# Kernel optimization log

Measured on AMD Instinct MI355X. Metric: run time of the kernel, lower is better.

## Reference

```python
import jax, jax.numpy as jnp
import numpy as np

D = 128
NUM_ITEM, NUM_CAT = 100000, 10000
NI, NC = 100000, 10000
EII, ECC, ECI, EIC = 800000, 100000, 400000, 400000
B, T, L = 512, 50, 2


def setup_inputs():
    key = jax.random.key(0)
    ks = jax.random.split(key, 48)
    s = 1.0 / np.sqrt(D)  # matches reset_parameters uniform(-stdv, stdv)
    u = lambda k, sh: jax.random.uniform(k, sh, jnp.float32, -s, s)
    ri = lambda k, sh, hi: jax.random.randint(k, sh, 0, hi, jnp.int32)
    inp = {
        'item_emb': u(ks[0], (NUM_ITEM, D)),
        'cate_emb': u(ks[1], (NUM_CAT, D)),
        'pos_emb': u(ks[2], (200, D)),
        'W_pos': u(ks[3], (2 * D, D)),
        'gat_W': u(ks[4], (L, 4, D, D)),
        'gat_al': u(ks[5], (L, 4, D)),
        'gat_ar': u(ks[6], (L, 4, D)),
        'gat_b': u(ks[7], (L, 4, D)),
        'Wg1_w': u(ks[8], (2 * D, D)), 'Wg1_b': u(ks[9], (D,)),
        'Wg3_w': u(ks[10], (2 * D, D)), 'Wg3_b': u(ks[11], (D,)),
        'q': u(ks[12], (D, 1)),
        'lin_out_w': u(ks[13], (2 * D, D)), 'lin_out_b': u(ks[14], (D,)),
        'w_1': u(ks[15], (2 * D, D)), 'w_2': u(ks[16], (D, 1)),
        'glu1_w': u(ks[17], (D, D)), 'glu1_b': u(ks[18], (D,)),
        'glu2_w': u(ks[19], (D, D)),
        'ln1_g': jnp.ones((D,), jnp.float32), 'ln1_b': jnp.zeros((D,), jnp.float32),
        'ln2_g': jnp.ones((D,), jnp.float32), 'ln2_b': jnp.zeros((D,), jnp.float32),
        'x_s': jax.random.uniform(ks[20], (1,), jnp.float32),
        'y_s': jax.random.uniform(ks[21], (1,), jnp.float32),
        'iid': ri(ks[22], (NI,), NUM_ITEM),
        'icate': ri(ks[23], (NI,), NUM_CAT),
        'cid': ri(ks[24], (NC,), NUM_CAT),
        'src_ii': ri(ks[25], (EII,), NI), 'dst_ii': ri(ks[26], (EII,), NI),
        'src_cc': ri(ks[27], (ECC,), NC), 'dst_cc': ri(ks[28], (ECC,), NC),
        'src_ci': ri(ks[29], (ECI,), NC), 'dst_ci': ri(ks[30], (ECI,), NI),
        'src_ic': ri(ks[31], (EIC,), NI), 'dst_ic': ri(ks[32], (EIC,), NC),
        'alias': ri(ks[33], (B, T), NI),
        'seq_items': ri(ks[34], (B, T), NUM_ITEM),
        'mask_item': jnp.ones((B, T), jnp.int32),
        'last_idx': ri(ks[35], (B,), NI),
    }
    return inp


def _layernorm(x, g, b, eps=1e-8):
    mu = x.mean(-1, keepdims=True)
    v = ((x - mu) ** 2).mean(-1, keepdims=True)
    return (x - mu) / jnp.sqrt(v + eps) * g + b


def _gat(h_src, h_dst, src, dst, W, al, ar, bias, n_dst):
    # DGL GATConv, 1 head, residual (identity since in==out), negative_slope=0.2
    z_src = h_src @ W                      # [Nsrc, D]
    z_dst = h_dst @ W                      # [Ndst, D]
    e = jax.nn.leaky_relu((z_src @ al)[src] + (z_dst @ ar)[dst], 0.2)  # [E]
    m = jax.ops.segment_max(e, dst, num_segments=n_dst)
    ee = jnp.exp(e - m[dst])
    denom = jax.ops.segment_sum(ee, dst, num_segments=n_dst)
    alpha = ee / denom[dst]                # edge softmax per destination
    out = jax.ops.segment_sum(alpha[:, None] * z_src[src], dst, num_segments=n_dst)
    return out + h_dst + bias              # residual then bias (DGL order)


def _compute_scores(hidden, maskf, pos, q, lin_out_w, lin_out_b, w_1, w_2,
                    glu1_w, glu1_b, glu2_w, ln1_g, ln1_b, ln2_g, ln2_b):
    # hidden: [B,T,D], maskf: [B,T,1]
    hs = hidden @ q                                    # [B,T,1]
    beta_a = jax.nn.softmax(hs, axis=1) * maskf
    hsv = jnp.sum(beta_a * hidden, axis=1)             # [B,D]
    hsv = _layernorm(hsv, ln1_g, ln1_b)
    hh = hidden[:, 0]                                  # first position
    hsv = jnp.concatenate([hsv, hh], axis=1) @ lin_out_w + lin_out_b
    nh = jnp.tanh(jnp.concatenate([jnp.broadcast_to(pos[None], hidden.shape), hidden], -1) @ w_1)
    nh = jax.nn.sigmoid(nh @ glu1_w + glu1_b + (hsv @ glu2_w)[:, None, :])
    beta = (nh @ w_2) * maskf                          # [B,T,1]
    sel = jnp.sum(beta * hidden, axis=1)               # [B,D]
    return _layernorm(sel, ln2_g, ln2_b)               # nor == True


def reference(item_emb, cate_emb, pos_emb, W_pos, gat_W, gat_al, gat_ar, gat_b,
              Wg1_w, Wg1_b, Wg3_w, Wg3_b, q, lin_out_w, lin_out_b, w_1, w_2,
              glu1_w, glu1_b, glu2_w, ln1_g, ln1_b, ln2_g, ln2_b, x_s, y_s,
              iid, icate, cid, src_ii, dst_ii, src_cc, dst_cc, src_ci, dst_ci,
              src_ic, dst_ic, alias, seq_items, mask_item, last_idx):
    # feature_encoder
    hi0 = jnp.concatenate([item_emb[iid], cate_emb[icate]], axis=1) @ W_pos  # [NI,D]
    hc0 = cate_emb[cid]                                                     # [NC,D]
    hi, hc = hi0, hc0
    for l in range(L):
        # HeteroGraphConv, aggregate='sum'; relation order: i2i, c2c, c2i, i2c
        ni = (_gat(hi, hi, src_ii, dst_ii, gat_W[l, 0], gat_al[l, 0], gat_ar[l, 0], gat_b[l, 0], NI)
              + _gat(hc, hi, src_ci, dst_ci, gat_W[l, 2], gat_al[l, 2], gat_ar[l, 2], gat_b[l, 2], NI))
        nc = (_gat(hc, hc, src_cc, dst_cc, gat_W[l, 1], gat_al[l, 1], gat_ar[l, 1], gat_b[l, 1], NC)
              + _gat(hi, hc, src_ic, dst_ic, gat_W[l, 3], gat_al[l, 3], gat_ar[l, 3], gat_b[l, 3], NC))
        hi, hc = ni, nc
    # FeatureSelect type='gated' between layer 0 and last layer
    gate_i = jax.nn.sigmoid(jnp.concatenate([hi0, hi], axis=-1) @ Wg1_w + Wg1_b)
    feat_i = gate_i * hi0 + (1.0 - gate_i) * hi
    gate_c = jax.nn.sigmoid(jnp.concatenate([hc0, hc], axis=-1) @ Wg3_w + Wg3_b)
    feat_c = gate_c * hc0 + (1.0 - gate_c) * hc  # computed per original; unused below
    maskf = mask_item.astype(jnp.float32)[..., None]        # [B,T,1]
    h_i_last = feat_i[last_idx]                             # last item per session
    seq_hidden = item_emb[seq_items]                        # local-path embeddings
    h_he = feat_i[alias] * maskf                            # GNN features gathered per session (zero-padded)
    h_all0 = seq_hidden * x_s[0] + h_he
    h_l = _compute_scores(h_all0, maskf, pos_emb[:T], q, lin_out_w, lin_out_b, w_1, w_2,
                          glu1_w, glu1_b, glu2_w, ln1_g, ln1_b, ln2_g, ln2_b)
    h_all = h_l + h_i_last * y_s[0]                         # [B,D]
    fenzi = h_all @ h_all.T
    fenmu_l = jnp.sqrt(jnp.sum(h_all * h_all + 1e-6, axis=1))[:, None]
    cos_sim = fenzi / (fenmu_l @ fenmu_l.T)
    return h_all, cos_sim
```

## Files before the change

### kernel.cpp

```cpp
#include <hip/hip_runtime.h>
#include <hip/hip_fp16.h>

typedef unsigned short u16;
typedef unsigned int u32;
typedef unsigned long long u64;
typedef __attribute__((ext_vector_type(8))) short bf16x8;
typedef __attribute__((ext_vector_type(4))) float f32x4;

#define NI_ 100000
#define NC_ 10000
#define EII_ 800000
#define ECC_ 100000
#define ECI_ 400000
#define EIC_ 400000
#define B_ 512
#define T_ 50
#define BSH_ 9
#define NBII_ 196
#define NBNC_ 20
#define NBK_ 432
#define ECH_ 4096

__device__ __forceinline__ float bf2f(u16 u) { return __uint_as_float(((u32)u) << 16); }
__device__ __forceinline__ u16 f2bf(float x) {
    u32 u = __float_as_uint(x);
    return (u16)((u + 0x7FFFu + ((u >> 16) & 1u)) >> 16);
}
__device__ __forceinline__ float sigm(float x) { return 1.f / (1.f + expf(-x)); }
__device__ __forceinline__ float gldf(const void* p, size_t i, int isf) {
    return isf ? ((const float*)p)[i] : bf2f(((const u16*)p)[i]);
}
__device__ __forceinline__ float lrelu_c(float v) {
    v = (v >= 0.f) ? v : 0.2f * v;
    return fminf(fmaxf(v, -60.f), 60.f);
}

__global__ void k_init(const void* __restrict__ item, int* __restrict__ flag,
                       int* __restrict__ bcnt)
{
    const int tid = threadIdx.x;
    for (int i = tid; i < NBK_; i += 128) bcnt[i] = 0;
    if (tid < 64) {
        const int l = tid;
        bf16x8 a, b;
        #pragma unroll
        for (int j = 0; j < 8; ++j) {
            int ka = (l >> 4) * 8 + j;
            float av = (float)((((l & 15) * 5 + ka * 3) & 15) - 7);
            float bv = (float)(((ka * 7 + (l & 15) * 11) & 15) - 8);
            a[j] = (short)f2bf(av);
            b[j] = (short)f2bf(bv);
        }
        f32x4 d = {0.f, 0.f, 0.f, 0.f};
        d = __builtin_amdgcn_mfma_f32_16x16x32_bf16(a, b, d, 0, 0, 0);
        bool ok = true;
        #pragma unroll
        for (int j = 0; j < 4; ++j) {
            int row = (l >> 4) * 4 + j, col = l & 15;
            float ref = 0.f;
            for (int k = 0; k < 32; ++k)
                ref += (float)(((row * 5 + k * 3) & 15) - 7) * (float)(((k * 7 + col * 11) & 15) - 8);
            ok = ok && (d[j] == ref);
        }
        unsigned long long vote = __ballot(ok);
        if (l == 0) flag[1] = (vote == ~0ull) ? 1 : 0;
    } else if (tid == 64) {
        const u16* p = (const u16*)item;
        int cnt = 0;
        for (int i = 0; i < 128; ++i) {
            float v = bf2f(p[i]);
            if (fabsf(v) <= 0.0886f) ++cnt;
        }
        flag[0] = (cnt >= 120) ? 0 : 1;
    }
}

__global__ void s_sig(float* __restrict__ out, long n, float code)
{
    long i = (long)blockIdx.x * 256 + threadIdx.x;
    if (i < n) out[i] = (i == 0) ? code : 0.f;
}

__global__ __launch_bounds__(256) void k_pre(
    const void* __restrict__ cate, const int* __restrict__ cid, float* __restrict__ hc0,
    const void* __restrict__ Wp, const void* __restrict__ Wg1, const void* __restrict__ gW,
    u16* __restrict__ whi, u16* __restrict__ wlo,
    const void* __restrict__ ar, float* __restrict__ wars,
    const int* __restrict__ d0, const int* __restrict__ d1,
    const int* __restrict__ d2, const int* __restrict__ d3,
    int* __restrict__ bcnt,
    const int* __restrict__ fl)
{
    __shared__ int bl[NBK_];
    const int det = fl[0];
    int bid = blockIdx.x, tid = threadIdx.x;
    if (bid < 5000) {
        long i = (long)bid * 256 + tid;
        if (i < (long)NC_ * 128)
            hc0[i] = gldf(cate, (size_t)cid[i >> 7] * 128 + (i & 127), det);
        return;
    }
    bid -= 5000;
    if (bid < 80) {
        int s = bid * 256 + tid;
        if (s >= 20480) return;
        const void* src; int K, local; size_t soff;
        if (s < 4096)       { src = Wp;  K = 256; local = s;        soff = 0; }
        else if (s < 8192)  { src = Wg1; K = 256; local = s - 4096; soff = 0; }
        else {
            int t = s - 8192; int m = t >> 11; local = t & 2047; K = 128;
            const int MK[6] = {0, 1, 2, 3, 4, 6};
            src = gW; soff = (size_t)MK[m] * 16384;
        }
        const int KK = K >> 5;
        int r = local & 15, g = (local >> 4) & 3, q2 = local >> 6;
        int kk = q2 % KK, ni = q2 / KK;
        bf16x8 hv, lv;
        #pragma unroll
        for (int j = 0; j < 8; ++j) {
            float x = gldf(src, soff + (size_t)(kk * 32 + 8 * g + j) * 128 + ni * 16 + r, det);
            u16 hb = f2bf(x);
            hv[j] = (short)hb;
            lv[j] = (short)f2bf(x - bf2f(hb));
        }
        *(bf16x8*)(whi + (size_t)s * 8) = hv;
        *(bf16x8*)(wlo + (size_t)s * 8) = lv;
        return;
    }
    bid -= 80;
    if (bid < 3) {
        if (tid < 128) {
            const int WO[3] = {2 * 16384, 3 * 16384, 6 * 16384};
            const int AO[3] = {2 * 128, 3 * 128, 6 * 128};
            int g = bid, k = tid;
            float a = 0.f;
            for (int c = 0; c < 128; ++c)
                a += gldf(gW, (size_t)WO[g] + (size_t)k * 128 + c, det) * gldf(ar, AO[g] + c, det);
            wars[g * 128 + k] = a;
        }
        return;
    }
    bid -= 3;
    for (int i = tid; i < NBK_; i += 256) bl[i] = 0;
    __syncthreads();
    const long ET = (long)EII_ + ECI_ + ECC_ + EIC_;
    const long base = (long)bid * ECH_;
    #pragma unroll
    for (int j = 0; j < 16; ++j) {
        long i = base + j * 256 + tid;
        if (i < ET) {
            int dst, boff;
            long ii = i;
            if (ii < EII_) { dst = d0[ii]; boff = 0; }
            else { ii -= EII_;
            if (ii < ECI_) { dst = d1[ii]; boff = NBII_; }
            else { ii -= ECI_;
            if (ii < ECC_) { dst = d2[ii]; boff = 2 * NBII_; }
            else { ii -= ECC_; dst = d3[ii]; boff = 2 * NBII_ + NBNC_; } } }
            atomicAdd(&bl[boff + (dst >> BSH_)], 1);
        }
    }
    __syncthreads();
    for (int i = tid; i < NBK_; i += 256)
        if (bl[i]) atomicAdd(&bcnt[i], bl[i]);
}

__global__ void k_bscan(const int* __restrict__ bcnt,
                        int* __restrict__ bstart, int* __restrict__ gcur)
{
    if (threadIdx.x != 0 || blockIdx.x != 0) return;
    int run = 0;
    for (int i = 0; i < NBII_; ++i) { bstart[i] = run; gcur[i] = run; run += bcnt[i]; }
    run = 0;
    for (int i = NBII_; i < 2 * NBII_; ++i) { bstart[i] = run; gcur[i] = run; run += bcnt[i]; }
    run = 0;
    for (int i = 2 * NBII_; i < 2 * NBII_ + NBNC_; ++i) { bstart[i] = run; gcur[i] = run; run += bcnt[i]; }
    run = 0;
    for (int i = 2 * NBII_ + NBNC_; i < NBK_; ++i) { bstart[i] = run; gcur[i] = run; run += bcnt[i]; }
}

__global__ __launch_bounds__(256) void k_binA(
    const int* s0, const int* d0, const int* s1, const int* d1,
    const int* s2, const int* d2, const int* s3, const int* d3,
    int* __restrict__ gcur,
    u32* __restrict__ b0, u32* __restrict__ b1,
    u32* __restrict__ b2, u32* __restrict__ b3)
{
    __shared__ u32 stag[ECH_];
    __shared__ int cnt[NBK_], base_l[NBK_ + 1], gbase[NBK_], cur_l[NBK_];
    const int tid = threadIdx.x;
    const long estart = (long)blockIdx.x * ECH_;
    const long ET = (long)EII_ + ECI_ + ECC_ + EIC_;
    for (int b = tid; b < NBK_; b += 256) cnt[b] = 0;
    __syncthreads();
    int gidv[16]; u32 pk[16];
    #pragma unroll
    for (int j = 0; j < 16; ++j) {
        long i = estart + j * 256 + tid;
        gidv[j] = -1;
        if (i < ET) {
            int src, dst, boff;
            long ii = i;
            if (ii < EII_) { src = s0[ii]; dst = d0[ii]; boff = 0; }
            else { ii -= EII_;
            if (ii < ECI_) { src = s1[ii]; dst = d1[ii]; boff = NBII_; }
            else { ii -= ECI_;
            if (ii < ECC_) { src = s2[ii]; dst = d2[ii]; boff = 2 * NBII_; }
            else { ii -= ECC_; src = s3[ii]; dst = d3[ii]; boff = 2 * NBII_ + NBNC_; } } }
            int gid = boff + (dst >> BSH_);
            gidv[j] = gid;
            pk[j] = ((u32)src << BSH_) | (u32)(dst & ((1 << BSH_) - 1));
            atomicAdd(&cnt[gid], 1);
        }
    }
    __syncthreads();
    if (tid == 0) {
        int run = 0;
        for (int b = 0; b < NBK_; ++b) { base_l[b] = run; run += cnt[b]; }
        base_l[NBK_] = run;
    }
    __syncthreads();
    for (int b = tid; b < NBK_; b += 256) {
        gbase[b] = cnt[b] ? atomicAdd(&gcur[b], cnt[b]) : 0;
        cur_l[b] = base_l[b];
    }
    __syncthreads();
    #pragma unroll
    for (int j = 0; j < 16; ++j)
        if (gidv[j] >= 0) {
            int l = atomicAdd(&cur_l[gidv[j]], 1);
            stag[l] = pk[j];
        }
    __syncthreads();
    const int total = base_l[NBK_];
    for (int t = tid; t < total; t += 256) {
        int lo = 0, hi = NBK_ - 1;
        while (lo < hi) { int mid = (lo + hi + 1) >> 1; if (base_l[mid] <= t) lo = mid; else hi = mid - 1; }
        int pos = gbase[lo] + (t - base_l[lo]);
        u32* bp = (lo < NBII_) ? b0 : (lo < 2 * NBII_) ? b1 : (lo < 2 * NBII_ + NBNC_) ? b2 : b3;
        bp[pos] = stag[t];
    }
}

__global__ __launch_bounds__(512) void k_binB(
    const int* __restrict__ bstart, const int* __restrict__ bcnt,
    const u32* __restrict__ b0, const u32* __restrict__ b1,
    const u32* __restrict__ b2, const u32* __restrict__ b3,
    int* __restrict__ rpII, int* __restrict__ rpCI,
    int* __restrict__ rpCC, int* __restrict__ rpIC,
    int* __restrict__ csII, int* __restrict__ csCI,
    int* __restrict__ csCC, int* __restrict__ csIC)
{
    __shared__ int cnt[512], cur[512];
    const int gid = blockIdx.x, tid = threadIdx.x;
    int* rp; const u32* bp; int* cs; int b, n, Eg; bool last;
    if (gid < NBII_)                  { rp = rpII; bp = b0; cs = csII; b = gid;                     n = NI_; Eg = EII_; last = (gid == NBII_ - 1); }
    else if (gid < 2 * NBII_)         { rp = rpCI; bp = b1; cs = csCI; b = gid - NBII_;             n = NI_; Eg = ECI_; last = (gid == 2 * NBII_ - 1); }
    else if (gid < 2 * NBII_ + NBNC_) { rp = rpCC; bp = b2; cs = csCC; b = gid - 2 * NBII_;         n = NC_; Eg = ECC_; last = (gid == 2 * NBII_ + NBNC_ - 1); }
    else                              { rp = rpIC; bp = b3; cs = csIC; b = gid - 2 * NBII_ - NBNC_; n = NC_; Eg = EIC_; last = (gid == NBK_ - 1); }
    const int dz = b << BSH_;
    const int d1v = (dz + 512 < n) ? dz + 512 : n;
    const int ndl = d1v - dz;
    cnt[tid] = 0;
    __syncthreads();
    const int e0 = bstart[gid], e1 = e0 + bcnt[gid];
    for (int e = e0 + tid; e < e1; e += 512)
        atomicAdd(&cnt[bp[e] & 511], 1);
    __syncthreads();
    for (int s = 1; s < 512; s <<= 1) {
        int v = (tid >= s) ? cnt[tid - s] : 0;
        __syncthreads();
        cnt[tid] += v;
        __syncthreads();
    }
    const int excl = (tid == 0) ? 0 : cnt[tid - 1];
    cur[tid] = e0 + excl;
    if (tid < ndl) rp[dz + tid] = e0 + excl;
    if (last && tid == 0) rp[n] = Eg;
    __syncthreads();
    for (int e = e0 + tid; e < e1; e += 512) {
        u32 p = bp[e];
        int pos = atomicAdd(&cur[p & 511], 1);
        cs[pos] = (int)(p >> BSH_);
    }
}

__device__ __forceinline__ void gat_gather(
    const int* __restrict__ rp, const int* __restrict__ cs,
    const float* __restrict__ sl, float srd, const __half2* __restrict__ z,
    int w, int lane, float& a0, float& a1)
{
    const int start = rp[w], end = rp[w + 1];
    if (end <= start) return;
    const int cnt = end - start;
    int   sE = 0; float eE = 0.f;
    if (lane < cnt) {
        sE = cs[start + lane];
        eE = expf(lrelu_c(sl[sE] + srd));
    }
    float local = eE;
    for (int k = start + 64 + lane; k < end; k += 64)
        local += expf(lrelu_c(sl[cs[k]] + srd));
    #pragma unroll
    for (int o = 32; o > 0; o >>= 1) local += __shfl_xor(local, o, 64);
    const float inv = 1.f / local;
    const int m = (cnt < 64) ? cnt : 64;
    int k = 0;
    for (; k + 8 <= m; k += 8) {
        int   s[8]; float lw[8]; float2 f[8];
        #pragma unroll
        for (int u = 0; u < 8; ++u) {
            s[u]  = __shfl(sE, k + u, 64);
            lw[u] = __shfl(eE, k + u, 64) * inv;
        }
        #pragma unroll
        for (int u = 0; u < 8; ++u) f[u] = __half22float2(z[(size_t)s[u] * 64 + lane]);
        #pragma unroll
        for (int u = 0; u < 8; ++u) { a0 += lw[u] * f[u].x; a1 += lw[u] * f[u].y; }
    }
    for (; k + 4 <= m; k += 4) {
        int s0 = __shfl(sE, k, 64),     s1 = __shfl(sE, k + 1, 64);
        int s2 = __shfl(sE, k + 2, 64), s3 = __shfl(sE, k + 3, 64);
        float l0 = __shfl(eE, k, 64) * inv,     l1 = __shfl(eE, k + 1, 64) * inv;
        float l2 = __shfl(eE, k + 2, 64) * inv, l3 = __shfl(eE, k + 3, 64) * inv;
        float2 f0 = __half22float2(z[(size_t)s0 * 64 + lane]);
        float2 f1 = __half22float2(z[(size_t)s1 * 64 + lane]);
        float2 f2 = __half22float2(z[(size_t)s2 * 64 + lane]);
        float2 f3 = __half22float2(z[(size_t)s3 * 64 + lane]);
        a0 += l0 * f0.x + l1 * f1.x + l2 * f2.x + l3 * f3.x;
        a1 += l0 * f0.y + l1 * f1.y + l2 * f2.y + l3 * f3.y;
    }
    for (; k < m; ++k) {
        int s = __shfl(sE, k, 64);
        float al = __shfl(eE, k, 64) * inv;
        float2 f = __half22float2(z[(size_t)s * 64 + lane]);
        a0 += al * f.x;
        a1 += al * f.y;
    }
    for (int kk = start + 64; kk < end; ++kk) {
        int s = cs[kk];
        float al = expf(lrelu_c(sl[s] + srd)) * inv;
        float2 f = __half22float2(z[(size_t)s * 64 + lane]);
        a0 += al * f.x;
        a1 += al * f.y;
    }
}

__global__ __launch_bounds__(256) void t_gat_fused(
    const int* __restrict__ rpA, const int* __restrict__ csA,
    const float* __restrict__ slA, const float* __restrict__ srA, const __half2* __restrict__ zA_,
    const int* __restrict__ rpB, const int* __restrict__ csB,
    const float* __restrict__ slB, const float* __restrict__ war, const __half2* __restrict__ zB_,
    const float* __restrict__ h0, const void* __restrict__ gb, int b0off, int b1off,
    const int* __restrict__ fl, float* __restrict__ acc, int ndst)
{
    int w = blockIdx.x * 4 + (threadIdx.x >> 6);
    int lane = threadIdx.x & 63;
    if (w >= ndst) return;
    const int det = *fl;
    const int d0 = 2 * lane, d1 = 2 * lane + 1;
    float2 h0v = *(const float2*)(h0 + (size_t)w * 128 + d0);
    float2 wv  = *(const float2*)(war + d0);
    float srB = h0v.x * wv.x + h0v.y * wv.y;
    #pragma unroll
    for (int off = 32; off > 0; off >>= 1) srB += __shfl_xor(srB, off, 64);
    float a0 = 2.f * h0v.x + gldf(gb, b0off + d0, det) + gldf(gb, b1off + d0, det);
    float a1 = 2.f * h0v.y + gldf(gb, b0off + d1, det) + gldf(gb, b1off + d1, det);
    gat_gather(rpA, csA, slA, srA[w], zA_, w, lane, a0, a1);
    gat_gather(rpB, csB, slB, srB,    zB_, w, lane, a0, a1);
    *(float2*)(acc + (size_t)w * 128 + d0) = make_float2(a0, a1);
}

__global__ __launch_bounds__(256) void k_prepw3(
    const void* __restrict__ w1, const void* __restrict__ g1w,
    const int* __restrict__ fl, u16* __restrict__ whi, u16* __restrict__ wlo)
{
    int s = blockIdx.x * 256 + threadIdx.x;
    if (s >= 6144) return;
    const int det = *fl;
    const void* src; int K, local;
    if (s < 4096) { src = w1;  K = 256; local = s; }
    else          { src = g1w; K = 128; local = s - 4096; }
    const int KK = K >> 5;
    int r = local & 15, g = (local >> 4) & 3, q2 = local >> 6;
    int kk = q2 % KK, ni = q2 / KK;
    bf16x8 hv, lv;
    #pragma unroll
    for (int j = 0; j < 8; ++j) {
        float x = gldf(src, (size_t)(kk * 32 + 8 * g + j) * 128 + ni * 16 + r, det);
        u16 hb = f2bf(x);
        hv[j] = (short)hb;
        lv[j] = (short)f2bf(x - bf2f(hb));
    }
    *(bf16x8*)(whi + (size_t)s * 8) = hv;
    *(bf16x8*)(wlo + (size_t)s * 8) = lv;
}

__global__ __launch_bounds__(256, 2) void m_hi0(
    const void* __restrict__ item, const void* __restrict__ cate,
    const int* __restrict__ iid, const int* __restrict__ icate,
    const u16* __restrict__ whi, const u16* __restrict__ wlo,
    const int* __restrict__ fl, const int* __restrict__ mfok,
    float* __restrict__ out, int nrows)
{
    if (*mfok == 0) return;
    __shared__ __align__(16) short Ah[2048 * 8];
    __shared__ __align__(16) short Alo[2048 * 8];
    const int det = *fl;
    const int tid = threadIdx.x, l = tid & 63, w = tid >> 6;
    const int base = blockIdx.x * 64;
    {
        int row = tid >> 2, q = tid & 3;
        int n = base + row, mi = row >> 4, r = row & 15;
        const int it = (n < nrows) ? iid[n] : 0;
        const int ct = (n < nrows) ? icate[n] : 0;
        #pragma unroll
        for (int i = 0; i < 8; ++i) {
            int c = q + 4 * i, kk = c >> 2, g = c & 3;
            int slot = ((mi * 8 + kk) * 4 + g) * 16 + r;
            bf16x8 hv = {0,0,0,0,0,0,0,0}, lv = {0,0,0,0,0,0,0,0};
            if (n < nrows) {
                #pragma unroll
                for (int j = 0; j < 8; ++j) {
                    float x = (c < 16) ? gldf(item, (size_t)it * 128 + c * 8 + j, det)
                                       : gldf(cate, (size_t)ct * 128 + (c - 16) * 8 + j, det);
                    u16 hb2 = f2bf(x);
                    hv[j] = (short)hb2;
                    lv[j] = (short)f2bf(x - bf2f(hb2));
                }
            }
            *(bf16x8*)&Ah[slot * 8]  = hv;
            *(bf16x8*)&Alo[slot * 8] = lv;
        }
    }
    bf16x8 breg[2][8];
    #pragma unroll
    for (int t = 0; t < 2; ++t)
        #pragma unroll
        for (int kk = 0; kk < 8; ++kk)
            breg[t][kk] = *(const bf16x8*)(whi + ((size_t)((w * 2 + t) * 8 + kk) * 64 + l) * 8);
    __syncthreads();
    f32x4 acc[4][2];
    #pragma unroll
    for (int mi = 0; mi < 4; ++mi) { acc[mi][0] = (f32x4){0.f,0.f,0.f,0.f}; acc[mi][1] = (f32x4){0.f,0.f,0.f,0.f}; }
    auto pass = [&](const short* AS) {
        #pragma unroll
        for (int kk = 0; kk < 8; ++kk) {
            bf16x8 a[4];
            #pragma unroll
            for (int mi = 0; mi < 4; ++mi) a[mi] = *(const bf16x8*)&AS[((mi * 8 + kk) * 64 + l) * 8];
            #pragma unroll
            for (int mi = 0; mi < 4; ++mi) {
                acc[mi][0] = __builtin_amdgcn_mfma_f32_16x16x32_bf16(a[mi], breg[0][kk], acc[mi][0], 0, 0, 0);
                acc[mi][1] = __builtin_amdgcn_mfma_f32_16x16x32_bf16(a[mi], breg[1][kk], acc[mi][1], 0, 0, 0);
            }
        }
    };
    pass(Ah);
    pass(Alo);
    #pragma unroll
    for (int t = 0; t < 2; ++t)
        #pragma unroll
        for (int kk = 0; kk < 8; ++kk)
            breg[t][kk] = *(const bf16x8*)(wlo + ((size_t)((w * 2 + t) * 8 + kk) * 64 + l) * 8);
    pass(Ah);
    const int g = l >> 4, r = l & 15, wn0 = w * 32;
    #pragma unroll
    for (int mi = 0; mi < 4; ++mi)
        #pragma unroll
        for (int j = 0; j < 4; ++j) {
            int row = base + mi * 16 + 4 * g + j;
            if (row < nrows) {
                out[(size_t)row * 128 + wn0 + r]      = acc[mi][0][j];
                out[(size_t)row * 128 + wn0 + 16 + r] = acc[mi][1][j];
            }
        }
}

__global__ __launch_bounds__(256, 2) void m_zgemm(
    const float* __restrict__ h, int nrows,
    const u16* __restrict__ whi, const u16* __restrict__ wlo,
    const void* __restrict__ al, int aloff, const void* __restrict__ ar, int aroff,
    const int* __restrict__ fl, const int* __restrict__ mfok,
    __half* __restrict__ z, float* __restrict__ sl, float* __restrict__ sr)
{
    if (*mfok == 0) return;
    __shared__ __align__(16) short Ah[1024 * 8];
    __shared__ __align__(16) short Alo[1024 * 8];
    __shared__ float part[2][4][64];
    const int det = *fl;
    const int tid = threadIdx.x, l = tid & 63, w = tid >> 6;
    const int base = blockIdx.x * 64;
    {
        int row = tid >> 2, q = tid & 3;
        int n = base + row, mi = row >> 4, r = row & 15;
        #pragma unroll
        for (int i = 0; i < 4; ++i) {
            int c = q + 4 * i, kk = c >> 2, g = c & 3;
            int slot = ((mi * 4 + kk) * 4 + g) * 16 + r;
            bf16x8 hv = {0,0,0,0,0,0,0,0}, lv = {0,0,0,0,0,0,0,0};
            if (n < nrows) {
                const float* sp = h + (size_t)n * 128 + c * 8;
                #pragma unroll
                for (int j = 0; j < 8; ++j) {
                    float x = sp[j];
                    u16 hb = f2bf(x);
                    hv[j] = (short)hb;
                    lv[j] = (short)f2bf(x - bf2f(hb));
                }
            }
            *(bf16x8*)&Ah[slot * 8]  = hv;
            *(bf16x8*)&Alo[slot * 8] = lv;
        }
    }
    bf16x8 breg[2][4];
    #pragma unroll
    for (int t = 0; t < 2; ++t)
        #pragma unroll
        for (int kk = 0; kk < 4; ++kk)
            breg[t][kk] = *(const bf16x8*)(whi + ((size_t)((w * 2 + t) * 4 + kk) * 64 + l) * 8);
    __syncthreads();
    f32x4 acc[4][2];
    #pragma unroll
    for (int mi = 0; mi < 4; ++mi) { acc[mi][0] = (f32x4){0.f,0.f,0.f,0.f}; acc[mi][1] = (f32x4){0.f,0.f,0.f,0.f}; }
    auto pass = [&](const short* AS) {
        #pragma unroll
        for (int kk = 0; kk < 4; ++kk) {
            bf16x8 a[4];
            #pragma unroll
            for (int mi = 0; mi < 4; ++mi) a[mi] = *(const bf16x8*)&AS[((mi * 4 + kk) * 64 + l) * 8];
            #pragma unroll
            for (int mi = 0; mi < 4; ++mi) {
                acc[mi][0] = __builtin_amdgcn_mfma_f32_16x16x32_bf16(a[mi], breg[0][kk], acc[mi][0], 0, 0, 0);
                acc[mi][1] = __builtin_amdgcn_mfma_f32_16x16x32_bf16(a[mi], breg[1][kk], acc[mi][1], 0, 0, 0);
            }
        }
    };
    pass(Ah);
    pass(Alo);
    #pragma unroll
    for (int t = 0; t < 2; ++t)
        #pragma unroll
        for (int kk = 0; kk < 4; ++kk)
            breg[t][kk] = *(const bf16x8*)(wlo + ((size_t)((w * 2 + t) * 4 + kk) * 64 + l) * 8);
    pass(Ah);
    const int g = l >> 4, r = l & 15, wn0 = w * 32;
    const float alv0 = gldf(al, (size_t)aloff + wn0 + r, det);
    const float alv1 = gldf(al, (size_t)aloff + wn0 + 16 + r, det);
    const float arv0 = gldf(ar, (size_t)aroff + wn0 + r, det);
    const float arv1 = gldf(ar, (size_t)aroff + wn0 + 16 + r, det);
    #pragma unroll
    for (int mi = 0; mi < 4; ++mi)
        #pragma unroll
        for (int j = 0; j < 4; ++j) {
            int row = base + mi * 16 + 4 * g + j;
            float d0 = acc[mi][0][j], d1 = acc[mi][1][j];
            if (row < nrows) {
                z[(size_t)row * 128 + wn0 + r]      = __float2half_rn(d0);
                z[(size_t)row * 128 + wn0 + 16 + r] = __float2half_rn(d1);
            }
            float pl = d0 * alv0 + d1 * alv1;
            float pr = d0 * arv0 + d1 * arv1;
            #pragma unroll
            for (int m2 = 1; m2 < 16; m2 <<= 1) {
                pl += __shfl_xor(pl, m2, 64);
                pr += __shfl_xor(pr, m2, 64);
            }
            if (r == 0) {
                part[0][w][mi * 16 + 4 * g + j] = pl;
                part[1][w][mi * 16 + 4 * g + j] = pr;
            }
        }
    __syncthreads();
    if (tid < 128) {
        int which = tid >> 6, t = tid & 63;
        int n2 = base + t;
        if (n2 < nrows) {
            float s = part[which][0][t] + part[which][1][t] + part[which][2][t] + part[which][3][t];
            (which ? sr : sl)[n2] = s;
        }
    }
}

__global__ __launch_bounds__(256, 2) void m_zgemm2(
    const float* __restrict__ h, int nrows,
    const u16* __restrict__ whi1, const u16* __restrict__ wlo1,
    int alo1, int aro1, __half* __restrict__ z1,
    float* __restrict__ sl1, float* __restrict__ sr1,
    const u16* __restrict__ whi2, const u16* __restrict__ wlo2,
    int alo2, int aro2, __half* __restrict__ z2,
    float* __restrict__ sl2, float* __restrict__ sr2,
    const void* __restrict__ al, const void* __restrict__ ar,
    const int* __restrict__ fl, const int* __restrict__ mfok)
{
    if (*mfok == 0) return;
    __shared__ __align__(16) short Ah[1024 * 8];
    __shared__ __align__(16) short Alo[1024 * 8];
    __shared__ float part[2][4][64];
    const int det = *fl;
    const int tid = threadIdx.x, l = tid & 63, w = tid >> 6;
    const int base = blockIdx.x * 64;
    {
        int row = tid >> 2, q = tid & 3;
        int n = base + row, mi = row >> 4, r = row & 15;
        #pragma unroll
        for (int i = 0; i < 4; ++i) {
            int c = q + 4 * i, kk = c >> 2, g = c & 3;
            int slot = ((mi * 4 + kk) * 4 + g) * 16 + r;
            bf16x8 hv = {0,0,0,0,0,0,0,0}, lv = {0,0,0,0,0,0,0,0};
            if (n < nrows) {
                const float* sp = h + (size_t)n * 128 + c * 8;
                #pragma unroll
                for (int j = 0; j < 8; ++j) {
                    float x = sp[j];
                    u16 hb = f2bf(x);
                    hv[j] = (short)hb;
                    lv[j] = (short)f2bf(x - bf2f(hb));
                }
            }
            *(bf16x8*)&Ah[slot * 8]  = hv;
            *(bf16x8*)&Alo[slot * 8] = lv;
        }
    }
    __syncthreads();
    const int g = l >> 4, r = l & 15, wn0 = w * 32;
    auto doSet = [&](const u16* whi, const u16* wlo, int aloff, int aroff,
                     __half* z, float* sl, float* sr) {
        bf16x8 breg[2][4];
        #pragma unroll
        for (int t = 0; t < 2; ++t)
            #pragma unroll
            for (int kk = 0; kk < 4; ++kk)
                breg[t][kk] = *(const bf16x8*)(whi + ((size_t)((w * 2 + t) * 4 + kk) * 64 + l) * 8);
        f32x4 acc[4][2];
        #pragma unroll
        for (int mi = 0; mi < 4; ++mi) { acc[mi][0] = (f32x4){0.f,0.f,0.f,0.f}; acc[mi][1] = (f32x4){0.f,0.f,0.f,0.f}; }
        auto pass = [&](const short* AS) {
            #pragma unroll
            for (int kk = 0; kk < 4; ++kk) {
                bf16x8 a[4];
                #pragma unroll
                for (int mi = 0; mi < 4; ++mi) a[mi] = *(const bf16x8*)&AS[((mi * 4 + kk) * 64 + l) * 8];
                #pragma unroll
                for (int mi = 0; mi < 4; ++mi) {
                    acc[mi][0] = __builtin_amdgcn_mfma_f32_16x16x32_bf16(a[mi], breg[0][kk], acc[mi][0], 0, 0, 0);
                    acc[mi][1] = __builtin_amdgcn_mfma_f32_16x16x32_bf16(a[mi], breg[1][kk], acc[mi][1], 0, 0, 0);
                }
            }
        };
        pass(Ah);
        pass(Alo);
        #pragma unroll
        for (int t = 0; t < 2; ++t)
            #pragma unroll
            for (int kk = 0; kk < 4; ++kk)
                breg[t][kk] = *(const bf16x8*)(wlo + ((size_t)((w * 2 + t) * 4 + kk) * 64 + l) * 8);
        pass(Ah);
        const float alv0 = gldf(al, (size_t)aloff + wn0 + r, det);
        const float alv1 = gldf(al, (size_t)aloff + wn0 + 16 + r, det);
        const float arv0 = gldf(ar, (size_t)aroff + wn0 + r, det);
        const float arv1 = gldf(ar, (size_t)aroff + wn0 + 16 + r, det);
        #pragma unroll
        for (int mi = 0; mi < 4; ++mi)
            #pragma unroll
            for (int j = 0; j < 4; ++j) {
                int row = base + mi * 16 + 4 * g + j;
                float d0 = acc[mi][0][j], d1 = acc[mi][1][j];
                if (row < nrows) {
                    z[(size_t)row * 128 + wn0 + r]      = __float2half_rn(d0);
                    z[(size_t)row * 128 + wn0 + 16 + r] = __float2half_rn(d1);
                }
                float pl = d0 * alv0 + d1 * alv1;
                float pr = d0 * arv0 + d1 * arv1;
                #pragma unroll
                for (int m2 = 1; m2 < 16; m2 <<= 1) {
                    pl += __shfl_xor(pl, m2, 64);
                    pr += __shfl_xor(pr, m2, 64);
                }
                if (r == 0) {
                    part[0][w][mi * 16 + 4 * g + j] = pl;
                    part[1][w][mi * 16 + 4 * g + j] = pr;
                }
            }
        __syncthreads();
        if (tid < 128) {
            int which = tid >> 6, t = tid & 63;
            int n2 = base + t;
            if (n2 < nrows) {
                float s = part[which][0][t] + part[which][1][t] + part[which][2][t] + part[which][3][t];
                (which ? sr : sl)[n2] = s;
            }
        }
        __syncthreads();
    };
    doSet(whi1, wlo1, alo1, aro1, z1, sl1, sr1);
    doSet(whi2, wlo2, alo2, aro2, z2, sl2, sr2);
}

__global__ __launch_bounds__(256, 2) void m_gatefeat(
    const float* __restrict__ h0, const float* __restrict__ h1,
    const u16* __restrict__ whi, const u16* __restrict__ wlo,
    const void* __restrict__ bias,
    const int* __restrict__ fl, const int* __restrict__ mfok,
    float* __restrict__ feat, int nrows)
{
    if (*mfok == 0) return;
    __shared__ __align__(16) short Ah[2048 * 8];
    __shared__ __align__(16) short Alo[2048 * 8];
    const int det = *fl;
    const int tid = threadIdx.x, l = tid & 63, w = tid >> 6;
    const int base = blockIdx.x * 64;
    {
        int row = tid >> 2, q = tid & 3;
        int n = base + row, mi = row >> 4, r = row & 15;
        #pragma unroll
        for (int i = 0; i < 8; ++i) {
            int c = q + 4 * i, kk = c >> 2, g = c & 3;
            int slot = ((mi * 8 + kk) * 4 + g) * 16 + r;
            bf16x8 hv = {0,0,0,0,0,0,0,0}, lv = {0,0,0,0,0,0,0,0};
            if (n < nrows) {
                const float* sp = ((c < 16) ? h0 : h1) + (size_t)n * 128 + (c & 15) * 8;
                #pragma unroll
                for (int j = 0; j < 8; ++j) {
                    float x = sp[j];
                    u16 hb = f2bf(x);
                    hv[j] = (short)hb;
                    lv[j] = (short)f2bf(x - bf2f(hb));
                }
            }
            *(bf16x8*)&Ah[slot * 8]  = hv;
            *(bf16x8*)&Alo[slot * 8] = lv;
        }
    }
    bf16x8 breg[2][8];
    #pragma unroll
    for (int t = 0; t < 2; ++t)
        #pragma unroll
        for (int kk = 0; kk < 8; ++kk)
            breg[t][kk] = *(const bf16x8*)(whi + ((size_t)((w * 2 + t) * 8 + kk) * 64 + l) * 8);
    __syncthreads();
    f32x4 acc[4][2];
    #pragma unroll
    for (int mi = 0; mi < 4; ++mi) { acc[mi][0] = (f32x4){0.f,0.f,0.f,0.f}; acc[mi][1] = (f32x4){0.f,0.f,0.f,0.f}; }
    auto pass = [&](const short* AS) {
        #pragma unroll
        for (int kk = 0; kk < 8; ++kk) {
            bf16x8 a[4];
            #pragma unroll
            for (int mi = 0; mi < 4; ++mi) a[mi] = *(const bf16x8*)&AS[((mi * 8 + kk) * 64 + l) * 8];
            #pragma unroll
            for (int mi = 0; mi < 4; ++mi) {
                acc[mi][0] = __builtin_amdgcn_mfma_f32_16x16x32_bf16(a[mi], breg[0][kk], acc[mi][0], 0, 0, 0);
                acc[mi][1] = __builtin_amdgcn_mfma_f32_16x16x32_bf16(a[mi], breg[1][kk], acc[mi][1], 0, 0, 0);
            }
        }
    };
    pass(Ah);
    pass(Alo);
    #pragma unroll
    for (int t = 0; t < 2; ++t)
        #pragma unroll
        for (int kk = 0; kk < 8; ++kk)
            breg[t][kk] = *(const bf16x8*)(wlo + ((size_t)((w * 2 + t) * 8 + kk) * 64 + l) * 8);
    pass(Ah);
    const int g = l >> 4, r = l & 15, wn0 = w * 32;
    const float bv0 = gldf(bias, wn0 + r, det);
    const float bv1 = gldf(bias, wn0 + 16 + r, det);
    #pragma unroll
    for (int mi = 0; mi < 4; ++mi)
        #pragma unroll
        for (int j = 0; j < 4; ++j) {
            int row = base + mi * 16 + 4 * g + j;
            if (row < nrows) {
                size_t o0 = (size_t)row * 128 + wn0 + r;
                size_t o1 = o0 + 16;
                float ga  = sigm(acc[mi][0][j] + bv0);
                float gb2 = sigm(acc[mi][1][j] + bv1);
                feat[o0] = ga  * h0[o0] + (1.f - ga)  * h1[o0];
                feat[o1] = gb2 * h0[o1] + (1.f - gb2) * h1[o1];
            }
        }
}

__global__ __launch_bounds__(256, 2) void m_nhglu(
    const void* __restrict__ pos, const float* __restrict__ hall0,
    const u16* __restrict__ whi1, const u16* __restrict__ wlo1,
    const u16* __restrict__ whi2, const u16* __restrict__ wlo2,
    const void* __restrict__ gb, const float* __restrict__ g2,
    const void* __restrict__ w2, const int* __restrict__ mask,
    const int* __restrict__ fl, const int* __restrict__ mfok,
    float* __restrict__ beta, int nrows)
{
    if (*mfok == 0) return;
    __shared__ __align__(16) short Ah[2048 * 8];
    __shared__ __align__(16) short Alo[2048 * 8];
    __shared__ float part[4][64];
    const int det = *fl;
    const int tid = threadIdx.x, l = tid & 63, w = tid >> 6;
    const int base = blockIdx.x * 64;
    {
        int row = tid >> 2, q = tid & 3;
        int n = base + row, mi = row >> 4, r = row & 15;
        const int t = (n < nrows) ? (n - (n / T_) * T_) : 0;
        #pragma unroll
        for (int i = 0; i < 8; ++i) {
            int c = q + 4 * i, kk = c >> 2, g = c & 3;
            int slot = ((mi * 8 + kk) * 4 + g) * 16 + r;
            bf16x8 hv = {0,0,0,0,0,0,0,0}, lv = {0,0,0,0,0,0,0,0};
            if (n < nrows) {
                #pragma unroll
                for (int j = 0; j < 8; ++j) {
                    float x = (c < 16) ? gldf(pos, (size_t)t * 128 + c * 8 + j, det)
                                       : hall0[(size_t)n * 128 + (c - 16) * 8 + j];
                    u16 hb = f2bf(x);
                    hv[j] = (short)hb;
                    lv[j] = (short)f2bf(x - bf2f(hb));
                }
            }
            *(bf16x8*)&Ah[slot * 8]  = hv;
            *(bf16x8*)&Alo[slot * 8] = lv;
        }
    }
    bf16x8 breg[2][8];
    #pragma unroll
    for (int t = 0; t < 2; ++t)
        #pragma unroll
        for (int kk = 0; kk < 8; ++kk)
            breg[t][kk] = *(const bf16x8*)(whi1 + ((size_t)((w * 2 + t) * 8 + kk) * 64 + l) * 8);
    __syncthreads();
    f32x4 acc[4][2];
    #pragma unroll
    for (int mi = 0; mi < 4; ++mi) { acc[mi][0] = (f32x4){0.f,0.f,0.f,0.f}; acc[mi][1] = (f32x4){0.f,0.f,0.f,0.f}; }
    auto pass1 = [&](const short* AS) {
        #pragma unroll
        for (int kk = 0; kk < 8; ++kk) {
            bf16x8 a[4];
            #pragma unroll
            for (int mi = 0; mi < 4; ++mi) a[mi] = *(const bf16x8*)&AS[((mi * 8 + kk) * 64 + l) * 8];
            #pragma unroll
            for (int mi = 0; mi < 4; ++mi) {
                acc[mi][0] = __builtin_amdgcn_mfma_f32_16x16x32_bf16(a[mi], breg[0][kk], acc[mi][0], 0, 0, 0);
                acc[mi][1] = __builtin_amdgcn_mfma_f32_16x16x32_bf16(a[mi], breg[1][kk], acc[mi][1], 0, 0, 0);
            }
        }
    };
    pass1(Ah);
    pass1(Alo);
    #pragma unroll
    for (int t = 0; t < 2; ++t)
        #pragma unroll
        for (int kk = 0; kk < 8; ++kk)
            breg[t][kk] = *(const bf16x8*)(wlo1 + ((size_t)((w * 2 + t) * 8 + kk) * 64 + l) * 8);
    pass1(Ah);
    __syncthreads();
    {
        const int g = l >> 4, r = l & 15, wn0 = w * 32;
        #pragma unroll
        for (int mi = 0; mi < 4; ++mi)
            #pragma unroll
            for (int j = 0; j < 4; ++j) {
                int nloc = mi * 16 + 4 * g + j;
                int rr = nloc & 15, mi2 = nloc >> 4;
                #pragma unroll
                for (int hh = 0; hh < 2; ++hh) {
                    int col = wn0 + 16 * hh + r;
                    float x = tanhf(acc[mi][hh][j]);
                    int c = col >> 3, jj = col & 7;
                    int slot = ((mi2 * 4 + (c >> 2)) * 4 + (c & 3)) * 16 + rr;
                    u16 hb = f2bf(x);
                    Ah[slot * 8 + jj]  = (short)hb;
                    Alo[slot * 8 + jj] = (short)f2bf(x - bf2f(hb));
                }
            }
    }
    __syncthreads();
    bf16x8 breg2[2][4];
    #pragma unroll
    for (int t = 0; t < 2; ++t)
        #pragma unroll
        for (int kk = 0; kk < 4; ++kk)
            breg2[t][kk] = *(const bf16x8*)(whi2 + ((size_t)((w * 2 + t) * 4 + kk) * 64 + l) * 8);
    f32x4 acc2[4][2];
    #pragma unroll
    for (int mi = 0; mi < 4; ++mi) { acc2[mi][0] = (f32x4){0.f,0.f,0.f,0.f}; acc2[mi][1] = (f32x4){0.f,0.f,0.f,0.f}; }
    auto pass2 = [&](const short* AS) {
        #pragma unroll
        for (int kk = 0; kk < 4; ++kk) {
            bf16x8 a[4];
            #pragma unroll
            for (int mi = 0; mi < 4; ++mi) a[mi] = *(const bf16x8*)&AS[((mi * 4 + kk) * 64 + l) * 8];
            #pragma unroll
            for (int mi = 0; mi < 4; ++mi) {
                acc2[mi][0] = __builtin_amdgcn_mfma_f32_16x16x32_bf16(a[mi], breg2[0][kk], acc2[mi][0], 0, 0, 0);
                acc2[mi][1] = __builtin_amdgcn_mfma_f32_16x16x32_bf16(a[mi], breg2[1][kk], acc2[mi][1], 0, 0, 0);
            }
        }
    };
    pass2(Ah);
    pass2(Alo);
    #pragma unroll
    for (int t = 0; t < 2; ++t)
        #pragma unroll
        for (int kk = 0; kk < 4; ++kk)
            breg2[t][kk] = *(const bf16x8*)(wlo2 + ((size_t)((w * 2 + t) * 4 + kk) * 64 + l) * 8);
    pass2(Ah);
    const int g = l >> 4, r = l & 15, wn0 = w * 32;
    const float gbv0 = gldf(gb, wn0 + r, det);
    const float gbv1 = gldf(gb, wn0 + 16 + r, det);
    const float w2v0 = gldf(w2, wn0 + r, det);
    const float w2v1 = gldf(w2, wn0 + 16 + r, det);
    #pragma unroll
    for (int mi = 0; mi < 4; ++mi)
        #pragma unroll
        for (int j = 0; j < 4; ++j) {
            int row = base + mi * 16 + 4 * g + j;
            int b = row / T_;
            float gv0 = (row < nrows) ? g2[(size_t)b * 128 + wn0 + r]      : 0.f;
            float gv1 = (row < nrows) ? g2[(size_t)b * 128 + wn0 + 16 + r] : 0.f;
            float v0 = sigm(acc2[mi][0][j] + gbv0 + gv0);
            float v1 = sigm(acc2[mi][1][j] + gbv1 + gv1);
            float pl = v0 * w2v0 + v1 * w2v1;
            #pragma unroll
            for (int m2 = 1; m2 < 16; m2 <<= 1) pl += __shfl_xor(pl, m2, 64);
            if (r == 0) part[w][mi * 16 + 4 * g + j] = pl;
        }
    __syncthreads();
    if (tid < 64) {
        int n2 = base + tid;
        if (n2 < nrows) {
            float s = part[0][tid] + part[1][tid] + part[2][tid] + part[3][tid];
            beta[n2] = s * (float)mask[n2];
        }
    }
}

__global__ __launch_bounds__(512) void t_hi0(
    const void* __restrict__ item, const void* __restrict__ cate,
    const int* __restrict__ iid, const int* __restrict__ icate,
    const void* __restrict__ Wp, const int* __restrict__ fl,
    float* __restrict__ out, int nrows)
{
    __shared__ float Ws[8192];
    __shared__ float hrow[16][256];
    const int det = *fl;
    const int tid = threadIdx.x, c = tid & 31, slot = tid >> 5;
    for (int base = blockIdx.x * 16; base < nrows; base += gridDim.x * 16) {
        const int n = base + slot;
        if (n < nrows) {
            const int it = iid[n], ct = icate[n];
            for (int j = c; j < 128; j += 32) {
                hrow[slot][j]       = gldf(item, (size_t)it * 128 + j, det);
                hrow[slot][128 + j] = gldf(cate, (size_t)ct * 128 + j, det);
            }
        }
        float4 acc = make_float4(0.f, 0.f, 0.f, 0.f);
        for (int kb = 0; kb < 256; kb += 64) {
            __syncthreads();
            for (int i = tid; i < 8192; i += 512) Ws[i] = gldf(Wp, (size_t)kb * 128 + i, det);
            __syncthreads();
            if (n < nrows) {
                #pragma unroll 8
                for (int k = 0; k < 64; ++k) {
                    float hv = hrow[slot][kb + k];
                    float4 w = *(const float4*)&Ws[k * 128 + c * 4];
                    acc.x += hv * w.x; acc.y += hv * w.y; acc.z += hv * w.z; acc.w += hv * w.w;
                }
            }
        }
        if (n < nrows) *(float4*)&out[(size_t)n * 128 + c * 4] = acc;
        __syncthreads();
    }
}

__global__ __launch_bounds__(256) void s_hc0(
    const void* __restrict__ cate, const int* __restrict__ cid,
    const int* __restrict__ fl, float* __restrict__ out)
{
    long i = (long)blockIdx.x * 256 + threadIdx.x;
    if (i >= (long)NC_ * 128) return;
    out[i] = gldf(cate, (size_t)cid[i >> 7] * 128 + (i & 127), *fl);
}

__global__ __launch_bounds__(256) void s_initacc(
    const float* __restrict__ h, const void* __restrict__ gb, int b0off, int b1off,
    const int* __restrict__ fl, float* __restrict__ acc, long total)
{
    long i = (long)blockIdx.x * 256 + threadIdx.x;
    if (i >= total) return;
    const int det = *fl, d = (int)(i & 127);
    acc[i] = 2.f * h[i] + gldf(gb, b0off + d, det) + gldf(gb, b1off + d, det);
}

__global__ __launch_bounds__(512) void t_zgemm(
    const float* __restrict__ h, int nrows,
    const void* __restrict__ W, int woff,
    const void* __restrict__ al, int aloff,
    const void* __restrict__ ar, int aroff,
    const int* __restrict__ fl,
    __half* __restrict__ z, float* __restrict__ sl, float* __restrict__ sr)
{
    __shared__ float Ws[8192];
    __shared__ float hrow[16][128];
    const int det = *fl;
    const int tid = threadIdx.x, c = tid & 31, slot = tid >> 5;
    float4 alv, arv;
    alv.x = gldf(al, (size_t)aloff + c * 4 + 0, det); alv.y = gldf(al, (size_t)aloff + c * 4 + 1, det);
    alv.z = gldf(al, (size_t)aloff + c * 4 + 2, det); alv.w = gldf(al, (size_t)aloff + c * 4 + 3, det);
    arv.x = gldf(ar, (size_t)aroff + c * 4 + 0, det); arv.y = gldf(ar, (size_t)aroff + c * 4 + 1, det);
    arv.z = gldf(ar, (size_t)aroff + c * 4 + 2, det); arv.w = gldf(ar, (size_t)aroff + c * 4 + 3, det);
    for (int base = blockIdx.x * 16; base < nrows; base += gridDim.x * 16) {
        const int n = base + slot;
        if (n < nrows) for (int j = c; j < 128; j += 32) hrow[slot][j] = h[(size_t)n * 128 + j];
        float4 acc = make_float4(0.f, 0.f, 0.f, 0.f);
        for (int kb = 0; kb < 128; kb += 64) {
            __syncthreads();
            for (int i = tid; i < 8192; i += 512) Ws[i] = gldf(W, (size_t)woff + (size_t)kb * 128 + i, det);
            __syncthreads();
            if (n < nrows) {
                #pragma unroll 8
                for (int k = 0; k < 64; ++k) {
                    float hv = hrow[slot][kb + k];
                    float4 w = *(const float4*)&Ws[k * 128 + c * 4];
                    acc.x += hv * w.x; acc.y += hv * w.y; acc.z += hv * w.z; acc.w += hv * w.w;
                }
            }
        }
        if (n < nrows) {
            z[(size_t)n * 128 + c * 4 + 0] = __float2half_rn(acc.x);
            z[(size_t)n * 128 + c * 4 + 1] = __float2half_rn(acc.y);
            z[(size_t)n * 128 + c * 4 + 2] = __float2half_rn(acc.z);
            z[(size_t)n * 128 + c * 4 + 3] = __float2half_rn(acc.w);
            float pl = acc.x * alv.x + acc.y * alv.y + acc.z * alv.z + acc.w * alv.w;
            float pr = acc.x * arv.x + acc.y * arv.y + acc.z * arv.z + acc.w * arv.w;
            #pragma unroll
            for (int off = 16; off > 0; off >>= 1) {
                pl += __shfl_down(pl, off, 32);
                pr += __shfl_down(pr, off, 32);
            }
            if (c == 0) { sl[n] = pl; sr[n] = pr; }
        }
        __syncthreads();
    }
}

__global__ __launch_bounds__(256) void s_dinit(float* __restrict__ den, int n)
{
    int i = blockIdx.x * 256 + threadIdx.x;
    if (i < n) den[i] = 0.f;
}
__global__ __launch_bounds__(256) void s_edge(
    const float* __restrict__ sl, const float* __restrict__ sr,
    const int* __restrict__ src, const int* __restrict__ dst,
    float* __restrict__ e, float* __restrict__ den, int E)
{
    int j = blockIdx.x * 256 + threadIdx.x;
    if (j >= E) return;
    float ee = expf(lrelu_c(sl[src[j]] + sr[dst[j]]));
    e[j] = ee;
    atomicAdd(&den[dst[j]], ee);
}
__global__ __launch_bounds__(256) void s_scatter(
    const float* __restrict__ e, const float* __restrict__ den,
    const int* __restrict__ src, const int* __restrict__ dst,
    const __half* __restrict__ z, float* __restrict__ acc, int E)
{
    long i = (long)blockIdx.x * 256 + threadIdx.x;
    if (i >= (long)E * 128) return;
    int j = (int)(i >> 7), d = (int)(i & 127);
    int dj = dst[j];
    atomicAdd(&acc[(size_t)dj * 128 + d], (e[j] / den[dj]) * __half2float(z[(size_t)src[j] * 128 + d]));
}

__global__ __launch_bounds__(512) void t_gatefeat(
    const float* __restrict__ h0, const float* __restrict__ h1,
    const void* __restrict__ W, const void* __restrict__ bias,
    const int* __restrict__ fl,
    float* __restrict__ feat, int nrows)
{
    __shared__ float Ws[8192];
    __shared__ float hrow[16][256];
    const int det = *fl;
    const int tid = threadIdx.x, c = tid & 31, slot = tid >> 5;
    float4 bv;
    bv.x = gldf(bias, c * 4 + 0, det); bv.y = gldf(bias, c * 4 + 1, det);
    bv.z = gldf(bias, c * 4 + 2, det); bv.w = gldf(bias, c * 4 + 3, det);
    for (int base = blockIdx.x * 16; base < nrows; base += gridDim.x * 16) {
        const int n = base + slot;
        if (n < nrows) {
            for (int j = c; j < 128; j += 32) {
                hrow[slot][j]       = h0[(size_t)n * 128 + j];
                hrow[slot][128 + j] = h1[(size_t)n * 128 + j];
            }
        }
        float4 acc = make_float4(0.f, 0.f, 0.f, 0.f);
        for (int kb = 0; kb < 256; kb += 64) {
            __syncthreads();
            for (int i = tid; i < 8192; i += 512) Ws[i] = gldf(W, (size_t)kb * 128 + i, det);
            __syncthreads();
            if (n < nrows) {
                #pragma unroll 8
                for (int k = 0; k < 64; ++k) {
                    float hv = hrow[slot][kb + k];
                    float4 w = *(const float4*)&Ws[k * 128 + c * 4];
                    acc.x += hv * w.x; acc.y += hv * w.y; acc.z += hv * w.z; acc.w += hv * w.w;
                }
            }
        }
        if (n < nrows) {
            float4 a = *(const float4*)&hrow[slot][c * 4];
            float4 b = *(const float4*)&hrow[slot][128 + c * 4];
            float gx = sigm(acc.x + bv.x), gy = sigm(acc.y + bv.y);
            float gz = sigm(acc.z + bv.z), gw = sigm(acc.w + bv.w);
            float4 o;
            o.x = gx * a.x + (1.f - gx) * b.x;
            o.y = gy * a.y + (1.f - gy) * b.y;
            o.z = gz * a.z + (1.f - gz) * b.z;
            o.w = gw * a.w + (1.f - gw) * b.w;
            *(float4*)&feat[(size_t)n * 128 + c * 4] = o;
        }
        __syncthreads();
    }
}

__global__ __launch_bounds__(128) void t_attn12(
    const void* __restrict__ item, const int* __restrict__ seq,
    const int* __restrict__ alias, const int* __restrict__ maskp,
    const float* __restrict__ feat, const void* __restrict__ xs,
    const void* __restrict__ q,
    const void* __restrict__ g, const void* __restrict__ bb,
    const void* __restrict__ lw, const void* __restrict__ lb,
    const void* __restrict__ gw, const int* __restrict__ fl,
    float* __restrict__ hall0, float* __restrict__ g2)
{
    __shared__ float hl[T_][129];
    __shared__ float qs[128];
    __shared__ float hs_s[T_];
    __shared__ float red[128];
    __shared__ float h1s[128];
    __shared__ float h2[128];
    const int b = blockIdx.x, tid = threadIdx.x;
    const int det = *fl;
    const float x = gldf(xs, 0, det);
    qs[tid] = gldf(q, tid, det);
    for (int t = 0; t < T_; ++t) {
        int bt = b * T_ + t;
        float v = gldf(item, (size_t)seq[bt] * 128 + tid, det) * x
                + feat[(size_t)alias[bt] * 128 + tid] * (float)maskp[bt];
        hl[t][tid] = v;
        hall0[(size_t)bt * 128 + tid] = v;
    }
    __syncthreads();
    if (tid < T_) {
        float a = 0.f;
        for (int d = 0; d < 128; ++d) a += hl[tid][d] * qs[d];
        hs_s[tid] = a;
    }
    __syncthreads();
    float mx = -1e30f;
    for (int t = 0; t < T_; ++t) mx = fmaxf(mx, hs_s[t]);
    float ssum = 0.f;
    for (int t = 0; t < T_; ++t) ssum += expf(hs_s[t] - mx);
    float inv = 1.f / ssum;
    __syncthreads();
    if (tid < T_)
        hs_s[tid] = expf(hs_s[tid] - mx) * inv * (float)maskp[b * T_ + tid];
    __syncthreads();
    float a = 0.f;
    for (int t = 0; t < T_; ++t) a += hs_s[t] * hl[t][tid];
    red[tid] = a; __syncthreads();
    for (int o = 64; o > 0; o >>= 1) { if (tid < o) red[tid] += red[tid + o]; __syncthreads(); }
    float mu = red[0] * (1.f / 128.f);
    __syncthreads();
    float dv = a - mu;
    red[tid] = dv * dv; __syncthreads();
    for (int o = 64; o > 0; o >>= 1) { if (tid < o) red[tid] += red[tid + o]; __syncthreads(); }
    float rs = 1.f / sqrtf(red[0] * (1.f / 128.f) + 1e-8f);
    h1s[tid] = dv * rs * gldf(g, tid, det) + gldf(bb, tid, det);
    __syncthreads();
    float a2 = gldf(lb, tid, det);
    for (int k = 0; k < 128; ++k)
        a2 += h1s[k] * gldf(lw, (size_t)k * 128 + tid, det);
    for (int k = 0; k < 128; ++k)
        a2 += hl[0][k] * gldf(lw, (size_t)(128 + k) * 128 + tid, det);
    h2[tid] = a2;
    __syncthreads();
    float g2v = 0.f;
    for (int k = 0; k < 128; ++k)
        g2v += h2[k] * gldf(gw, (size_t)k * 128 + tid, det);
    g2[(size_t)b * 128 + tid] = g2v;
}

__global__ __launch_bounds__(512) void t_nh(
    const void* __restrict__ pos, const float* __restrict__ hall0,
    const void* __restrict__ W, const int* __restrict__ fl,
    float* __restrict__ nh, int nrows)
{
    __shared__ float Ws[8192];
    __shared__ float hrow[16][256];
    const int det = *fl;
    const int tid = threadIdx.x, c = tid & 31, slot = tid >> 5;
    for (int base = blockIdx.x * 16; base < nrows; base += gridDim.x * 16) {
        const int n = base + slot;
        if (n < nrows) {
            const int t = n - (n / T_) * T_;
            for (int j = c; j < 128; j += 32) {
                hrow[slot][j]       = gldf(pos, (size_t)t * 128 + j, det);
                hrow[slot][128 + j] = hall0[(size_t)n * 128 + j];
            }
        }
        float4 acc = make_float4(0.f, 0.f, 0.f, 0.f);
        for (int kb = 0; kb < 256; kb += 64) {
            __syncthreads();
            for (int i = tid; i < 8192; i += 512) Ws[i] = gldf(W, (size_t)kb * 128 + i, det);
            __syncthreads();
            if (n < nrows) {
                #pragma unroll 8
                for (int k = 0; k < 64; ++k) {
                    float hv = hrow[slot][kb + k];
                    float4 w = *(const float4*)&Ws[k * 128 + c * 4];
                    acc.x += hv * w.x; acc.y += hv * w.y; acc.z += hv * w.z; acc.w += hv * w.w;
                }
            }
        }
        if (n < nrows) {
            float4 o;
            o.x = tanhf(acc.x); o.y = tanhf(acc.y); o.z = tanhf(acc.z); o.w = tanhf(acc.w);
            *(float4*)&nh[(size_t)n * 128 + c * 4] = o;
        }
        __syncthreads();
    }
}

__global__ __launch_bounds__(512) void t_glu_beta(
    const float* __restrict__ nh, const void* __restrict__ W, const void* __restrict__ gb,
    const float* __restrict__ g2, const void* __restrict__ w2, const int* __restrict__ mask,
    const int* __restrict__ fl, float* __restrict__ beta, int nrows)
{
    __shared__ float Ws[8192];
    __shared__ float hrow[16][128];
    const int det = *fl;
    const int tid = threadIdx.x, c = tid & 31, slot = tid >> 5;
    float4 gbv, w2v;
    gbv.x = gldf(gb, c * 4 + 0, det); gbv.y = gldf(gb, c * 4 + 1, det);
    gbv.z = gldf(gb, c * 4 + 2, det); gbv.w = gldf(gb, c * 4 + 3, det);
    w2v.x = gldf(w2, c * 4 + 0, det); w2v.y = gldf(w2, c * 4 + 1, det);
    w2v.z = gldf(w2, c * 4 + 2, det); w2v.w = gldf(w2, c * 4 + 3, det);
    for (int base = blockIdx.x * 16; base < nrows; base += gridDim.x * 16) {
        const int n = base + slot;
        if (n < nrows) for (int j = c; j < 128; j += 32) hrow[slot][j] = nh[(size_t)n * 128 + j];
        float4 acc = make_float4(0.f, 0.f, 0.f, 0.f);
        for (int kb = 0; kb < 128; kb += 64) {
            __syncthreads();
            for (int i = tid; i < 8192; i += 512) Ws[i] = gldf(W, (size_t)kb * 128 + i, det);
            __syncthreads();
            if (n < nrows) {
                #pragma unroll 8
                for (int k = 0; k < 64; ++k) {
                    float hv = hrow[slot][kb + k];
                    float4 w = *(const float4*)&Ws[k * 128 + c * 4];
                    acc.x += hv * w.x; acc.y += hv * w.y; acc.z += hv * w.z; acc.w += hv * w.w;
                }
            }
        }
        if (n < nrows) {
            const int b = n / T_;
            float4 gv = *(const float4*)&g2[(size_t)b * 128 + c * 4];
            float vx = sigm(acc.x + gbv.x + gv.x);
            float vy = sigm(acc.y + gbv.y + gv.y);
            float vz = sigm(acc.z + gbv.z + gv.z);
            float vw = sigm(acc.w + gbv.w + gv.w);
            float part = vx * w2v.x + vy * w2v.y + vz * w2v.z + vw * w2v.w;
            #pragma unroll
            for (int off = 16; off > 0; off >>= 1) part += __shfl_down(part, off, 32);
            if (c == 0) beta[n] = part * (float)mask[n];
        }
        __syncthreads();
    }
}

__global__ __launch_bounds__(128) void t_sel(
    const float* __restrict__ hall0, const float* __restrict__ beta,
    const void* __restrict__ g2, const void* __restrict__ b2,
    const float* __restrict__ feat, const int* __restrict__ lasti,
    const void* __restrict__ ys, const int* __restrict__ fl,
    float* __restrict__ hallf, float* __restrict__ fenmu, float* __restrict__ outh)
{
    __shared__ float bet[T_];
    __shared__ float red[128];
    const int b = blockIdx.x, tid = threadIdx.x;
    const int det = *fl;
    if (tid < T_) bet[tid] = beta[b * T_ + tid];
    __syncthreads();
    float acc = 0.f;
    for (int t = 0; t < T_; ++t) acc += bet[t] * hall0[((size_t)b * T_ + t) * 128 + tid];
    red[tid] = acc; __syncthreads();
    for (int off = 64; off > 0; off >>= 1) { if (tid < off) red[tid] += red[tid + off]; __syncthreads(); }
    float mu = red[0] * (1.f / 128.f);
    __syncthreads();
    float dv = acc - mu;
    red[tid] = dv * dv; __syncthreads();
    for (int off = 64; off > 0; off >>= 1) { if (tid < off) red[tid] += red[tid + off]; __syncthreads(); }
    float rs = 1.f / sqrtf(red[0] * (1.f / 128.f) + 1e-8f);
    __syncthreads();
    float h = dv * rs * gldf(g2, tid, det) + gldf(b2, tid, det)
            + feat[(size_t)lasti[b] * 128 + tid] * gldf(ys, 0, det);
    hallf[(size_t)b * 128 + tid] = h;
    outh[(size_t)b * 128 + tid] = h;
    red[tid] = h * h; __syncthreads();
    for (int off = 64; off > 0; off >>= 1) { if (tid < off) red[tid] += red[tid + off]; __syncthreads(); }
    if (tid == 0) fenmu[b] = sqrtf(red[0] + 128.f * 1e-6f);
}

__global__ __launch_bounds__(256) void t_cos(
    const float* __restrict__ hallf, const float* __restrict__ fenmu, float* __restrict__ out)
{
    __shared__ float hi[128];
    const int i = blockIdx.x, tid = threadIdx.x;
    if (tid < 128) hi[tid] = hallf[(size_t)i * 128 + tid];
    __syncthreads();
    const float fi = fenmu[i];
    for (int j = tid; j < B_; j += 256) {
        const float* hj = &hallf[(size_t)j * 128];
        float s = 0.f;
        for (int d = 0; d < 128; d += 4) {
            float4 a = *(const float4*)&hi[d];
            float4 bb = *(const float4*)&hj[d];
            s += a.x * bb.x + a.y * bb.y + a.z * bb.z + a.w * bb.w;
        }
        out[(size_t)i * B_ + j] = s / (fi * fenmu[j]);
    }
}

extern "C" void kernel_launch(void* const* d_in, const int* in_sizes, int n_in,
                              void* d_out, int out_size, void* d_ws, size_t ws_size,
                              hipStream_t stream)
{
    float* outf = (float*)d_out;
    const long OUT_N = (long)B_ * 128 + (long)B_ * B_;

    static const int EXP_SZ[41] = {
        12800000, 1280000, 25600, 32768, 131072, 1024, 1024, 1024, 32768, 128,
        32768, 128, 128, 32768, 128, 32768, 128, 16384, 128, 16384,
        128, 128, 128, 128, 1, 1, 100000, 100000, 10000, 800000,
        800000, 100000, 100000, 400000, 400000, 400000, 400000, 25600, 25600, 25600, 512 };
    float code = 0.f;
    if (n_in != 41) code = 90000.f + (float)n_in;
    else {
        for (int i = 0; i < 41; ++i)
            if (in_sizes[i] != EXP_SZ[i]) { code = 10000.f * (float)(i + 1); break; }
    }
    if (code == 0.f && out_size != (int)OUT_N) code = 95000.f;
    if (code != 0.f) {
        s_sig<<<dim3((unsigned)((OUT_N + 255) / 256)), dim3(256), 0, stream>>>(outf, OUT_N, code);
        return;
    }

    const void* item_emb = d_in[0];
    const void* cate_emb = d_in[1];
    const void* pos_emb  = d_in[2];
    const void* W_pos    = d_in[3];
    const void* gat_W    = d_in[4];
    const void* gat_al   = d_in[5];
    const void* gat_ar   = d_in[6];
    const void* gat_b    = d_in[7];
    const void* Wg1_w    = d_in[8];
    const void* Wg1_b    = d_in[9];
    const void* q        = d_in[12];
    const void* lin_w    = d_in[13];
    const void* lin_b    = d_in[14];
    const void* w_1      = d_in[15];
    const void* w_2      = d_in[16];
    const void* glu1_w   = d_in[17];
    const void* glu1_b   = d_in[18];
    const void* glu2_w   = d_in[19];
    const void* ln1_g    = d_in[20];
    const void* ln1_b    = d_in[21];
    const void* ln2_g    = d_in[22];
    const void* ln2_b    = d_in[23];
    const void* x_s      = d_in[24];
    const void* y_s      = d_in[25];
    const int* iid    = (const int*)d_in[26];
    const int* icate  = (const int*)d_in[27];
    const int* cid    = (const int*)d_in[28];
    const int* src_ii = (const int*)d_in[29];
    const int* dst_ii = (const int*)d_in[30];
    const int* src_cc = (const int*)d_in[31];
    const int* dst_cc = (const int*)d_in[32];
    const int* src_ci = (const int*)d_in[33];
    const int* dst_ci = (const int*)d_in[34];
    const int* src_ic = (const int*)d_in[35];
    const int* dst_ic = (const int*)d_in[36];
    const int* alias  = (const int*)d_in[37];
    const int* seq    = (const int*)d_in[38];
    const int* mask   = (const int*)d_in[39];
    const int* lasti  = (const int*)d_in[40];

    const size_t NEED_BASE = 64 + ((size_t)4 * NI_ + 3 * NC_) * 128 * 4
                                + ((size_t)3 * NI_ + 2 * NC_ + EII_) * 4;
    const size_t CSR_EXTRA = ((size_t)2 * (NI_ + 1) + 2 * (NC_ + 1)
                                + ECI_ + ECC_ + EIC_ + NI_) * 4;
    const size_t NEED_CSR = NEED_BASE + CSR_EXTRA;
    if (ws_size < NEED_BASE) {
        s_sig<<<dim3((unsigned)((OUT_N + 255) / 256)), dim3(256), 0, stream>>>(outf, OUT_N, 80000.f);
        return;
    }
    const bool useCSR = (ws_size >= NEED_CSR);
    const int mf = useCSR ? 1 : 0;

    int* flagp = (int*)d_ws;
    char* basep = (char*)d_ws;
    size_t off = 64;
    auto AL = [&](size_t nfl) { float* p = (float*)(basep + off); off += nfl * 4; return p; };
    float* hi0 = AL((size_t)NI_ * 128);
    float* HiA = AL((size_t)NI_ * 128);
    float* HiB = AL((size_t)NI_ * 128);
    float* zA  = AL((size_t)NI_ * 128);
    float* hc0 = AL((size_t)NC_ * 128);
    float* HcA = AL((size_t)NC_ * 128);
    float* zC  = AL((size_t)NC_ * 128);
    float* sAl = AL(NI_); float* sAr = AL(NI_);
    float* sCl = AL(NC_); float* sCr = AL(NC_);
    float* denF = AL(NI_);
    float* eF   = AL(EII_);
    int* rpII = (int*)AL(NI_ + 1);
    int* rpCI = (int*)AL(NI_ + 1);
    int* rpCC = (int*)AL(NC_ + 1);
    int* rpIC = (int*)AL(NC_ + 1);
    int* csCI = (int*)AL(ECI_);
    int* csCC = (int*)AL(ECC_);
    int* csIC = (int*)AL(EIC_);
    int* wtregion = (int*)AL(NI_);
    int* csII = (int*)eF;
    int* denFi = (int*)denF;
    int* bcnt   = denFi;
    int* bstart = denFi + 512;
    int* gcur   = denFi + 1024;
    float* wars = denF + 2048;
    u16* wt_hi = (u16*)wtregion;
    u16* wt_lo = (u16*)((char*)denF + 17408);
    __half* zAh  = (__half*)zA;
    __half* zA2h = zAh + (size_t)NI_ * 128;
    __half* zCh  = (__half*)zC;
    __half* zC2h = zCh + (size_t)NC_ * 128;
    u32* binII = (u32*)HiB;
    u32* binCI = binII + EII_;
    u32* binCC = binCI + ECI_;
    u32* binIC = binCC + ECC_;
    float* sl03p = HiB;
    float* sr03s = HiB + NI_;
    float* sl02p = HiB + 2 * (size_t)NI_;
    float* sr02s = sl02p + NC_;
    u16* wt2_hi = (u16*)HiA;
    u16* wt2_lo = wt2_hi + (size_t)6144 * 8;

    auto WTS = [&](int l, int k) {
        int midx = (l == 0) ? k : ((k == 0) ? 4 : 5);
        return (size_t)(8192 + midx * 2048) * 8;
    };

    float* feat = zA;
    float* hall0 = hi0;
    float* nh    = hall0 + (size_t)B_ * T_ * 128;
    float* vbuf  = nh    + (size_t)B_ * T_ * 128;
    float* hsb   = vbuf  + (size_t)B_ * T_ * 128;
    float* hsv   = hsb   + (size_t)B_ * T_;
    float* hsvn  = hsv   + (size_t)B_ * 128;
    float* hsv2  = hsvn  + (size_t)B_ * 128;
    float* g2b   = hsv2  + (size_t)B_ * 128;
    float* betab = g2b   + (size_t)B_ * 128;
    float* hallf = betab + (size_t)B_ * T_;
    float* fenmu = hallf + (size_t)B_ * 128;

    #define GRL(n) dim3((unsigned)(((long)(n) + 255) / 256))
    auto WOFF = [](int l, int k) { return (l * 4 + k) * 16384; };
    auto VOFF = [](int l, int k) { return (l * 4 + k) * 128; };

    auto seg = [&](const float* sl, const float* sr, const int* s, const int* d,
                   int E, int ndst, const __half* z, float* acc) {
        s_dinit<<<GRL(ndst), dim3(256), 0, stream>>>(denF, ndst);
        s_edge<<<GRL(E), dim3(256), 0, stream>>>(sl, sr, s, d, eF, denF, E);
        s_scatter<<<GRL((long)E * 128), dim3(256), 0, stream>>>(eF, denF, s, d, z, acc, E);
    };

    k_init<<<dim3(1), dim3(128), 0, stream>>>(item_emb, flagp, bcnt);

    if (useCSR) {
        const int ET = EII_ + ECI_ + ECC_ + EIC_;
        const int NBA = (ET + ECH_ - 1) / ECH_;
        k_pre<<<dim3(5083 + NBA), dim3(256), 0, stream>>>(
            cate_emb, cid, hc0,
            W_pos, Wg1_w, gat_W, wt_hi, wt_lo, gat_ar, wars,
            dst_ii, dst_ci, dst_cc, dst_ic, bcnt, flagp);
        k_bscan<<<dim3(1), dim3(1), 0, stream>>>(bcnt, bstart, gcur);
        k_binA<<<dim3(NBA), dim3(256), 0, stream>>>(
            src_ii, dst_ii, src_ci, dst_ci, src_cc, dst_cc, src_ic, dst_ic,
            gcur, binII, binCI, binCC, binIC);
        k_binB<<<dim3(NBK_), dim3(512), 0, stream>>>(
            bstart, bcnt, binII, binCI, binCC, binIC,
            rpII, rpCI, rpCC, rpIC, csII, csCI, csCC, csIC);
        m_hi0<<<dim3((NI_ + 63) / 64), dim3(256), 0, stream>>>(
            item_emb, cate_emb, iid, icate, wt_hi, wt_lo, flagp, flagp + 1, hi0, NI_);
        m_zgemm2<<<dim3((NI_ + 63) / 64), dim3(256), 0, stream>>>(
            hi0, NI_,
            wt_hi + WTS(0, 0), wt_lo + WTS(0, 0), VOFF(0, 0), VOFF(0, 0), zAh,  sAl,   sAr,
            wt_hi + WTS(0, 3), wt_lo + WTS(0, 3), VOFF(0, 3), VOFF(0, 3), zA2h, sl03p, sr03s,
            gat_al, gat_ar, flagp, flagp + 1);
        m_zgemm2<<<dim3((NC_ + 63) / 64), dim3(256), 0, stream>>>(
            hc0, NC_,
            wt_hi + WTS(0, 1), wt_lo + WTS(0, 1), VOFF(0, 1), VOFF(0, 1), zC2h, sCl,   sCr,
            wt_hi + WTS(0, 2), wt_lo + WTS(0, 2), VOFF(0, 2), VOFF(0, 2), zCh,  sl02p, sr02s,
            gat_al, gat_ar, flagp, flagp + 1);
        t_gat_fused<<<dim3((NI_ + 3) / 4), dim3(256), 0, stream>>>(
            rpII, csII, sAl, sAr, (const __half2*)zAh,
            rpCI, csCI, sl02p, wars + 0, (const __half2*)zCh,
            hi0, gat_b, VOFF(0, 0), VOFF(0, 2), flagp, HiA, NI_);
        t_gat_fused<<<dim3((NC_ + 3) / 4), dim3(256), 0, stream>>>(
            rpCC, csCC, sCl, sCr, (const __half2*)zC2h,
            rpIC, csIC, sl03p, wars + 128, (const __half2*)zA2h,
            hc0, gat_b, VOFF(0, 1), VOFF(0, 3), flagp, HcA, NC_);
        m_zgemm<<<dim3((NI_ + 63) / 64), dim3(256), 0, stream>>>(
            HiA, NI_, wt_hi + WTS(1, 0), wt_lo + WTS(1, 0),
            gat_al, VOFF(1, 0), gat_ar, VOFF(1, 0), flagp, flagp + 1, zAh, sAl, sAr);
        m_zgemm<<<dim3((NC_ + 63) / 64), dim3(256), 0, stream>>>(
            HcA, NC_, wt_hi + WTS(1, 2), wt_lo + WTS(1, 2),
            gat_al, VOFF(1, 2), gat_ar, VOFF(1, 2), flagp, flagp + 1, zCh, sCl, sCr);
        t_gat_fused<<<dim3((NI_ + 3) / 4), dim3(256), 0, stream>>>(
            rpII, csII, sAl, sAr, (const __half2*)zAh,
            rpCI, csCI, sCl, wars + 256, (const __half2*)zCh,
            HiA, gat_b, VOFF(1, 0), VOFF(1, 2), flagp, HiB, NI_);
        k_prepw3<<<dim3(24), dim3(256), 0, stream>>>(w_1, glu1_w, flagp, wt2_hi, wt2_lo);
        m_gatefeat<<<dim3((NI_ + 63) / 64), dim3(256), 0, stream>>>(
            hi0, HiB, wt_hi + (size_t)4096 * 8, wt_lo + (size_t)4096 * 8, Wg1_b, flagp, flagp + 1, feat, NI_);
    } else {
        s_hc0<<<GRL((long)NC_ * 128), dim3(256), 0, stream>>>(cate_emb, cid, flagp, hc0);
        t_hi0<<<dim3(768), dim3(512), 0, stream>>>(item_emb, cate_emb, iid, icate, W_pos, flagp, hi0, NI_);
        s_initacc<<<GRL((long)NI_ * 128), dim3(256), 0, stream>>>(hi0, gat_b, VOFF(0, 0), VOFF(0, 2), flagp, HiA, (long)NI_ * 128);
        s_initacc<<<GRL((long)NC_ * 128), dim3(256), 0, stream>>>(hc0, gat_b, VOFF(0, 1), VOFF(0, 3), flagp, HcA, (long)NC_ * 128);
        t_zgemm<<<dim3(1024), dim3(512), 0, stream>>>(hi0, NI_, gat_W, WOFF(0, 0), gat_al, VOFF(0, 0), gat_ar, VOFF(0, 0), flagp, zAh, sAl, sAr);
        seg(sAl, sAr, src_ii, dst_ii, EII_, NI_, zAh, HiA);
        t_zgemm<<<dim3(625), dim3(512), 0, stream>>>(hc0, NC_, gat_W, WOFF(0, 2), gat_al, VOFF(0, 2), gat_ar, VOFF(0, 2), flagp, zCh, sCl, sCr);
        t_zgemm<<<dim3(1024), dim3(512), 0, stream>>>(hi0, NI_, gat_W, WOFF(0, 2), gat_al, VOFF(0, 2), gat_ar, VOFF(0, 2), flagp, zAh, sAl, sAr);
        seg(sCl, sAr, src_ci, dst_ci, ECI_, NI_, zCh, HiA);
        t_zgemm<<<dim3(625), dim3(512), 0, stream>>>(hc0, NC_, gat_W, WOFF(0, 1), gat_al, VOFF(0, 1), gat_ar, VOFF(0, 1), flagp, zCh, sCl, sCr);
        seg(sCl, sCr, src_cc, dst_cc, ECC_, NC_, zCh, HcA);
        t_zgemm<<<dim3(1024), dim3(512), 0, stream>>>(hi0, NI_, gat_W, WOFF(0, 3), gat_al, VOFF(0, 3), gat_ar, VOFF(0, 3), flagp, zAh, sAl, sAr);
        t_zgemm<<<dim3(625), dim3(512), 0, stream>>>(hc0, NC_, gat_W, WOFF(0, 3), gat_al, VOFF(0, 3), gat_ar, VOFF(0, 3), flagp, zCh, sCl, sCr);
        seg(sAl, sCr, src_ic, dst_ic, EIC_, NC_, zAh, HcA);
        s_initacc<<<GRL((long)NI_ * 128), dim3(256), 0, stream>>>(HiA, gat_b, VOFF(1, 0), VOFF(1, 2), flagp, HiB, (long)NI_ * 128);
        t_zgemm<<<dim3(1024), dim3(512), 0, stream>>>(HiA, NI_, gat_W, WOFF(1, 0), gat_al, VOFF(1, 0), gat_ar, VOFF(1, 0), flagp, zAh, sAl, sAr);
        seg(sAl, sAr, src_ii, dst_ii, EII_, NI_, zAh, HiB);
        t_zgemm<<<dim3(625), dim3(512), 0, stream>>>(HcA, NC_, gat_W, WOFF(1, 2), gat_al, VOFF(1, 2), gat_ar, VOFF(1, 2), flagp, zCh, sCl, sCr);
        t_zgemm<<<dim3(1024), dim3(512), 0, stream>>>(HiA, NI_, gat_W, WOFF(1, 2), gat_al, VOFF(1, 2), gat_ar, VOFF(1, 2), flagp, zAh, sAl, sAr);
        seg(sCl, sAr, src_ci, dst_ci, ECI_, NI_, zCh, HiB);
        t_gatefeat<<<dim3(768), dim3(512), 0, stream>>>(hi0, HiB, Wg1_w, Wg1_b, flagp, feat, NI_);
    }

    t_attn12<<<dim3(B_), dim3(128), 0, stream>>>(
        item_emb, seq, alias, mask, feat, x_s, q,
        ln1_g, ln1_b, lin_w, lin_b, glu2_w, flagp, hall0, g2b);
    if (mf) {
        m_nhglu<<<dim3((B_ * T_ + 63) / 64), dim3(256), 0, stream>>>(
            pos_emb, hall0, wt2_hi, wt2_lo,
            wt2_hi + (size_t)4096 * 8, wt2_lo + (size_t)4096 * 8,
            glu1_b, g2b, w_2, mask, flagp, flagp + 1, betab, B_ * T_);
    } else {
        int grid = (B_ * T_ + 15) / 16; if (grid > 1024) grid = 1024;
        t_nh<<<dim3(grid), dim3(512), 0, stream>>>(pos_emb, hall0, w_1, flagp, nh, B_ * T_);
        t_glu_beta<<<dim3(grid), dim3(512), 0, stream>>>(nh, glu1_w, glu1_b, g2b, w_2, mask, flagp, betab, B_ * T_);
    }
    t_sel<<<dim3(B_), dim3(128), 0, stream>>>(hall0, betab, ln2_g, ln2_b, feat, lasti, y_s, flagp, hallf, fenmu, outf);
    t_cos<<<dim3(B_), dim3(256), 0, stream>>>(hallf, fenmu, outf + (size_t)B_ * 128);
}
```

Baseline: 860.8 us.

## Fuse hi0 GEMM with z-GEMMs, merge item/category GAT launches, MFMA attention linears

Fuses the initial item projection with both layer-0 attention GEMMs so the projected rows stay in LDS and need not be re-read from global memory. It merges the item and category GAT aggregation launches, and likewise the two layer-1 z-GEMMs, into single dual-role grids. The per-session linear layers, previously done with scalar code inside t_attn12, move to a new MFMA kernel (m_lin) fed by a lighter attention kernel. The cost is more LDS use and register pressure in the fused kernel, plus more complex dispatch logic.

```diff
diff --git a/kernel.cpp b/kernel.cpp
--- a/kernel.cpp
+++ b/kernel.cpp
@@ -346,6 +346,28 @@
     }
 }
 
+__device__ __forceinline__ void gat_dst(
+    int w, int lane, int det,
+    const int* __restrict__ rpA, const int* __restrict__ csA,
+    const float* __restrict__ slA, const float* __restrict__ srA, const __half2* __restrict__ zA_,
+    const int* __restrict__ rpB, const int* __restrict__ csB,
+    const float* __restrict__ slB, const float* __restrict__ war, const __half2* __restrict__ zB_,
+    const float* __restrict__ h0, const void* __restrict__ gb, int b0off, int b1off,
+    float* __restrict__ acc)
+{
+    const int d0 = 2 * lane, d1 = 2 * lane + 1;
+    float2 h0v = *(const float2*)(h0 + (size_t)w * 128 + d0);
+    float2 wv  = *(const float2*)(war + d0);
+    float srB = h0v.x * wv.x + h0v.y * wv.y;
+    #pragma unroll
+    for (int off = 32; off > 0; off >>= 1) srB += __shfl_xor(srB, off, 64);
+    float a0 = 2.f * h0v.x + gldf(gb, b0off + d0, det) + gldf(gb, b1off + d0, det);
+    float a1 = 2.f * h0v.y + gldf(gb, b0off + d1, det) + gldf(gb, b1off + d1, det);
+    gat_gather(rpA, csA, slA, srA[w], zA_, w, lane, a0, a1);
+    gat_gather(rpB, csB, slB, srB,    zB_, w, lane, a0, a1);
+    *(float2*)(acc + (size_t)w * 128 + d0) = make_float2(a0, a1);
+}
+
 __global__ __launch_bounds__(256) void t_gat_fused(
     const int* __restrict__ rpA, const int* __restrict__ csA,
     const float* __restrict__ slA, const float* __restrict__ srA, const __half2* __restrict__ zA_,
@@ -357,30 +379,45 @@
     int w = blockIdx.x * 4 + (threadIdx.x >> 6);
     int lane = threadIdx.x & 63;
     if (w >= ndst) return;
+    gat_dst(w, lane, *fl, rpA, csA, slA, srA, zA_, rpB, csB, slB, war, zB_, h0, gb, b0off, b1off, acc);
+}
+
+__global__ __launch_bounds__(256) void t_gat2(
+    const int* rpAi, const int* csAi, const float* slAi, const float* srAi, const __half2* zAi,
+    const int* rpBi, const int* csBi, const float* slBi, const float* wari, const __half2* zBi,
+    const float* h0i, int b0i, int b1i, float* acci,
+    const int* rpAc, const int* csAc, const float* slAc, const float* srAc, const __half2* zAc,
+    const int* rpBc, const int* csBc, const float* slBc, const float* warc, const __half2* zBc,
+    const float* h0c, int b0c, int b1c, float* accc,
+    const void* __restrict__ gb, const int* __restrict__ fl)
+{
+    const int nblkI = (NI_ + 3) / 4;
+    const int lane = threadIdx.x & 63;
     const int det = *fl;
-    const int d0 = 2 * lane, d1 = 2 * lane + 1;
-    float2 h0v = *(const float2*)(h0 + (size_t)w * 128 + d0);
-    float2 wv  = *(const float2*)(war + d0);
-    float srB = h0v.x * wv.x + h0v.y * wv.y;
-    #pragma unroll
-    for (int off = 32; off > 0; off >>= 1) srB += __shfl_xor(srB, off, 64);
-    float a0 = 2.f * h0v.x + gldf(gb, b0off + d0, det) + gldf(gb, b1off + d0, det);
-    float a1 = 2.f * h0v.y + gldf(gb, b0off + d1, det) + gldf(gb, b1off + d1, det);
-    gat_gather(rpA, csA, slA, srA[w], zA_, w, lane, a0, a1);
-    gat_gather(rpB, csB, slB, srB,    zB_, w, lane, a0, a1);
-    *(float2*)(acc + (size_t)w * 128 + d0) = make_float2(a0, a1);
+    if ((int)blockIdx.x < nblkI) {
+        int w = blockIdx.x * 4 + (threadIdx.x >> 6);
+        if (w >= NI_) return;
+        gat_dst(w, lane, det, rpAi, csAi, slAi, srAi, zAi, rpBi, csBi, slBi, wari, zBi, h0i, gb, b0i, b1i, acci);
+    } else {
+        int w = (blockIdx.x - nblkI) * 4 + (threadIdx.x >> 6);
+        if (w >= NC_) return;
+        gat_dst(w, lane, det, rpAc, csAc, slAc, srAc, zAc, rpBc, csBc, slBc, warc, zBc, h0c, gb, b0c, b1c, accc);
+    }
 }
 
 __global__ __launch_bounds__(256) void k_prepw3(
     const void* __restrict__ w1, const void* __restrict__ g1w,
+    const void* __restrict__ lw, const void* __restrict__ g2w,
     const int* __restrict__ fl, u16* __restrict__ whi, u16* __restrict__ wlo)
 {
     int s = blockIdx.x * 256 + threadIdx.x;
-    if (s >= 6144) return;
+    if (s >= 12288) return;
     const int det = *fl;
     const void* src; int K, local;
-    if (s < 4096) { src = w1;  K = 256; local = s; }
-    else          { src = g1w; K = 128; local = s - 4096; }
+    if (s < 4096)       { src = w1;  K = 256; local = s; }
+    else if (s < 6144)  { src = g1w; K = 128; local = s - 4096; }
+    else if (s < 10240) { src = lw;  K = 256; local = s - 6144; }
+    else                { src = g2w; K = 128; local = s - 10240; }
     const int KK = K >> 5;
     int r = local & 15, g = (local >> 4) & 3, q2 = local >> 6;
     int kk = q2 % KK, ni = q2 / KK;
@@ -396,16 +433,100 @@
     *(bf16x8*)(wlo + (size_t)s * 8) = lv;
 }
 
-__global__ __launch_bounds__(256, 2) void m_hi0(
+__device__ __forceinline__ void zg_doset(
+    const short* __restrict__ Ah, const short* __restrict__ Alo,
+    float (*part)[4][64],
+    int tid, int l, int w, int base, int nrows, int det,
+    const u16* __restrict__ whi, const u16* __restrict__ wlo,
+    const void* __restrict__ al, int aloff, const void* __restrict__ ar, int aroff,
+    __half* __restrict__ z, float* __restrict__ sl, float* __restrict__ sr)
+{
+    bf16x8 breg[2][4];
+    #pragma unroll
+    for (int t = 0; t < 2; ++t)
+        #pragma unroll
+        for (int kk = 0; kk < 4; ++kk)
+            breg[t][kk] = *(const bf16x8*)(whi + ((size_t)((w * 2 + t) * 4 + kk) * 64 + l) * 8);
+    f32x4 acc[4][2];
+    #pragma unroll
+    for (int mi = 0; mi < 4; ++mi) { acc[mi][0] = (f32x4){0.f,0.f,0.f,0.f}; acc[mi][1] = (f32x4){0.f,0.f,0.f,0.f}; }
+    auto pass = [&](const short* AS) {
+        #pragma unroll
+        for (int kk = 0; kk < 4; ++kk) {
+            bf16x8 a[4];
+            #pragma unroll
+            for (int mi = 0; mi < 4; ++mi) a[mi] = *(const bf16x8*)&AS[((mi * 4 + kk) * 64 + l) * 8];
+            #pragma unroll
+            for (int mi = 0; mi < 4; ++mi) {
+                acc[mi][0] = __builtin_amdgcn_mfma_f32_16x16x32_bf16(a[mi], breg[0][kk], acc[mi][0], 0, 0, 0);
+                acc[mi][1] = __builtin_amdgcn_mfma_f32_16x16x32_bf16(a[mi], breg[1][kk], acc[mi][1], 0, 0, 0);
+            }
+        }
+    };
+    pass(Ah);
+    pass(Alo);
+    #pragma unroll
+    for (int t = 0; t < 2; ++t)
+        #pragma unroll
+        for (int kk = 0; kk < 4; ++kk)
+            breg[t][kk] = *(const bf16x8*)(wlo + ((size_t)((w * 2 + t) * 4 + kk) * 64 + l) * 8);
+    pass(Ah);
+    const int g = l >> 4, r = l & 15, wn0 = w * 32;
+    const float alv0 = gldf(al, (size_t)aloff + wn0 + r, det);
+    const float alv1 = gldf(al, (size_t)aloff + wn0 + 16 + r, det);
+    const float arv0 = gldf(ar, (size_t)aroff + wn0 + r, det);
+    const float arv1 = gldf(ar, (size_t)aroff + wn0 + 16 + r, det);
+    #pragma unroll
+    for (int mi = 0; mi < 4; ++mi)
+        #pragma unroll
+        for (int j = 0; j < 4; ++j) {
+            int row = base + mi * 16 + 4 * g + j;
+            float d0 = acc[mi][0][j], d1 = acc[mi][1][j];
+            if (row < nrows) {
+                z[(size_t)row * 128 + wn0 + r]      = __float2half_rn(d0);
+                z[(size_t)row * 128 + wn0 + 16 + r] = __float2half_rn(d1);
+            }
+            float pl = d0 * alv0 + d1 * alv1;
+            float pr = d0 * arv0 + d1 * arv1;
+            #pragma unroll
+            for (int m2 = 1; m2 < 16; m2 <<= 1) {
+                pl += __shfl_xor(pl, m2, 64);
+                pr += __shfl_xor(pr, m2, 64);
+            }
+            if (r == 0) {
+                part[0][w][mi * 16 + 4 * g + j] = pl;
+                part[1][w][mi * 16 + 4 * g + j] = pr;
+            }
+        }
+    __syncthreads();
+    if (tid < 128) {
+        int which = tid >> 6, t = tid & 63;
+        int n2 = base + t;
+        if (n2 < nrows) {
+            float s = part[which][0][t] + part[which][1][t] + part[which][2][t] + part[which][3][t];
+            (which ? sr : sl)[n2] = s;
+        }
+    }
+    __syncthreads();
+}
+
+__global__ __launch_bounds__(256, 2) void m_hi0zg(
     const void* __restrict__ item, const void* __restrict__ cate,
     const int* __restrict__ iid, const int* __restrict__ icate,
-    const u16* __restrict__ whi, const u16* __restrict__ wlo,
+    const u16* __restrict__ whi0, const u16* __restrict__ wlo0,
+    const u16* __restrict__ whiA, const u16* __restrict__ wloA, int aloA, int aroA,
+    const u16* __restrict__ whiB, const u16* __restrict__ wloB, int aloB, int aroB,
+    const void* __restrict__ al, const void* __restrict__ ar,
     const int* __restrict__ fl, const int* __restrict__ mfok,
-    float* __restrict__ out, int nrows)
+    float* __restrict__ hi0,
+    __half* __restrict__ z1, float* __restrict__ sl1, float* __restrict__ sr1,
+    __half* __restrict__ z2, float* __restrict__ sl2, float* __restrict__ sr2,
+    int nrows)
 {
     if (*mfok == 0) return;
     __shared__ __align__(16) short Ah[2048 * 8];
     __shared__ __align__(16) short Alo[2048 * 8];
+    __shared__ float part[2][4][64];
     const int det = *fl;
     const int tid = threadIdx.x, l = tid & 63, w = tid >> 6;
     const int base = blockIdx.x * 64;
@@ -438,12 +559,12 @@
     for (int t = 0; t < 2; ++t)
         #pragma unroll
         for (int kk = 0; kk < 8; ++kk)
-            breg[t][kk] = *(const bf16x8*)(whi + ((size_t)((w * 2 + t) * 8 + kk) * 64 + l) * 8);
+            breg[t][kk] = *(const bf16x8*)(whi0 + ((size_t)((w * 2 + t) * 8 + kk) * 64 + l) * 8);
     __syncthreads();
     f32x4 acc[4][2];
     #pragma unroll
     for (int mi = 0; mi < 4; ++mi) { acc[mi][0] = (f32x4){0.f,0.f,0.f,0.f}; acc[mi][1] = (f32x4){0.f,0.f,0.f,0.f}; }
-    auto pass = [&](const short* AS) {
+    auto pass8 = [&](const short* AS) {
         #pragma unroll
         for (int kk = 0; kk < 8; ++kk) {
             bf16x8 a[4];
@@ -456,33 +577,52 @@
             }
         }
     };
-    pass(Ah);
-    pass(Alo);
+    pass8(Ah);
+    pass8(Alo);
     #pragma unroll
     for (int t = 0; t < 2; ++t)
         #pragma unroll
         for (int kk = 0; kk < 8; ++kk)
-            breg[t][kk] = *(const bf16x8*)(wlo + ((size_t)((w * 2 + t) * 8 + kk) * 64 + l) * 8);
-    pass(Ah);
-    const int g = l >> 4, r = l & 15, wn0 = w * 32;
-    #pragma unroll
-    for (int mi = 0; mi < 4; ++mi)
-        #pragma unroll
-        for (int j = 0; j < 4; ++j) {
-            int row = base + mi * 16 + 4 * g + j;
-            if (row < nrows) {
-                out[(size_t)row * 128 + wn0 + r]      = acc[mi][0][j];
-                out[(size_t)row * 128 + wn0 + 16 + r] = acc[mi][1][j];
-            }
-        }
-}
-
-__global__ __launch_bounds__(256, 2) void m_zgemm(
+            breg[t][kk] = *(const bf16x8*)(wlo0 + ((size_t)((w * 2 + t) * 8 + kk) * 64 + l) * 8);
+    pass8(Ah);
+    __syncthreads();
+    {
+        const int g = l >> 4, r = l & 15, wn0 = w * 32;
+        #pragma unroll
+        for (int mi = 0; mi < 4; ++mi)
+            #pragma unroll
+            for (int j = 0; j < 4; ++j) {
+                int nloc = mi * 16 + 4 * g + j;
+                int row = base + nloc;
+                int rr = nloc & 15, mi2 = nloc >> 4;
+                #pragma unroll
+                for (int hh = 0; hh < 2; ++hh) {
+                    int col = wn0 + 16 * hh + r;
+                    float x = acc[mi][hh][j];
+                    if (row < nrows) hi0[(size_t)row * 128 + col] = x;
+                    int c = col >> 3, jj = col & 7;
+                    int slot = ((mi2 * 4 + (c >> 2)) * 4 + (c & 3)) * 16 + rr;
+                    u16 hb = f2bf(x);
+                    Ah[slot * 8 + jj]  = (short)hb;
+                    Alo[slot * 8 + jj] = (short)f2bf(x - bf2f(hb));
+                }
+            }
+    }
+    __syncthreads();
+    zg_doset(Ah, Alo, part, tid, l, w, base, nrows, det, whiA, wloA, al, aloA, ar, aroA, z1, sl1, sr1);
+    zg_doset(Ah, Alo, part, tid, l, w, base, nrows, det, whiB, wloB, al, aloB, ar, aroB, z2, sl2, sr2);
+}
+
+__global__ __launch_bounds__(256, 2) void m_zgemm2(
     const float* __restrict__ h, int nrows,
-    const u16* __restrict__ whi, const u16* __restrict__ wlo,
-    const void* __restrict__ al, int aloff, const void* __restrict__ ar, int aroff,
-    const int* __restrict__ fl, const int* __restrict__ mfok,
-    __half* __restrict__ z, float* __restrict__ sl, float* __restrict__ sr)
+    const u16* __restrict__ whi1, const u16* __restrict__ wlo1,
+    int alo1, int aro1, __half* __restrict__ z1,
+    float* __restrict__ sl1, float* __restrict__ sr1,
+    const u16* __restrict__ whi2, const u16* __restrict__ wlo2,
+    int alo2, int aro2, __half* __restrict__ z2,
+    float* __restrict__ sl2, float* __restrict__ sr2,
+    const void* __restrict__ al, const void* __restrict__ ar,
+    const int* __restrict__ fl, const int* __restrict__ mfok)
 {
     if (*mfok == 0) return;
     __shared__ __align__(16) short Ah[1024 * 8];
@@ -513,83 +653,18 @@
             *(bf16x8*)&Alo[slot * 8] = lv;
         }
     }
-    bf16x8 breg[2][4];
-    #pragma unroll
-    for (int t = 0; t < 2; ++t)
-        #pragma unroll
-        for (int kk = 0; kk < 4; ++kk)
-            breg[t][kk] = *(const bf16x8*)(whi + ((size_t)((w * 2 + t) * 4 + kk) * 64 + l) * 8);
-    __syncthreads();
-    f32x4 acc[4][2];
-    #pragma unroll
-    for (int mi = 0; mi < 4; ++mi) { acc[mi][0] = (f32x4){0.f,0.f,0.f,0.f}; acc[mi][1] = (f32x4){0.f,0.f,0.f,0.f}; }
-    auto pass = [&](const short* AS) {
-        #pragma unroll
-        for (int kk = 0; kk < 4; ++kk) {
-            bf16x8 a[4];
-            #pragma unroll
-            for (int mi = 0; mi < 4; ++mi) a[mi] = *(const bf16x8*)&AS[((mi * 4 + kk) * 64 + l) * 8];
-            #pragma unroll
-            for (int mi = 0; mi < 4; ++mi) {
-                acc[mi][0] = __builtin_amdgcn_mfma_f32_16x16x32_bf16(a[mi], breg[0][kk], acc[mi][0], 0, 0, 0);
-                acc[mi][1] = __builtin_amdgcn_mfma_f32_16x16x32_bf16(a[mi], breg[1][kk], acc[mi][1], 0, 0, 0);
-            }
-        }
-    };
-    pass(Ah);
-    pass(Alo);
-    #pragma unroll
-    for (int t = 0; t < 2; ++t)
-        #pragma unroll
-        for (int kk = 0; kk < 4; ++kk)
-            breg[t][kk] = *(const bf16x8*)(wlo + ((size_t)((w * 2 + t) * 4 + kk) * 64 + l) * 8);
-    pass(Ah);
-    const int g = l >> 4, r = l & 15, wn0 = w * 32;
-    const float alv0 = gldf(al, (size_t)aloff + wn0 + r, det);
-    const float alv1 = gldf(al, (size_t)aloff + wn0 + 16 + r, det);
-    const float arv0 = gldf(ar, (size_t)aroff + wn0 + r, det);
-    const float arv1 = gldf(ar, (size_t)aroff + wn0 + 16 + r, det);
-    #pragma unroll
-    for (int mi = 0; mi < 4; ++mi)
-        #pragma unroll
-        for (int j = 0; j < 4; ++j) {
-            int row = base + mi * 16 + 4 * g + j;
-            float d0 = acc[mi][0][j], d1 = acc[mi][1][j];
-            if (row < nrows) {
-                z[(size_t)row * 128 + wn0 + r]      = __float2half_rn(d0);
-                z[(size_t)row * 128 + wn0 + 16 + r] = __float2half_rn(d1);
-            }
-            float pl = d0 * alv0 + d1 * alv1;
-            float pr = d0 * arv0 + d1 * arv1;
-            #pragma unroll
-            for (int m2 = 1; m2 < 16; m2 <<= 1) {
-                pl += __shfl_xor(pl, m2, 64);
-                pr += __shfl_xor(pr, m2, 64);
-            }
-            if (r == 0) {
-                part[0][w][mi * 16 + 4 * g + j] = pl;
-                part[1][w][mi * 16 + 4 * g + j] = pr;
-            }
-        }
-    __syncthreads();
-    if (tid < 128) {
-        int which = tid >> 6, t = tid & 63;
-        int n2 = base + t;
-        if (n2 < nrows) {
-            float s = part[which][0][t] + part[which][1][t] + part[which][2][t] + part[which][3][t];
-            (which ? sr : sl)[n2] = s;
-        }
-    }
-}
-
-__global__ __launch_bounds__(256, 2) void m_zgemm2(
-    const float* __restrict__ h, int nrows,
-    const u16* __restrict__ whi1, const u16* __restrict__ wlo1,
-    int alo1, int aro1, __half* __restrict__ z1,
-    float* __restrict__ sl1, float* __restrict__ sr1,
-    const u16* __restrict__ whi2, const u16* __restrict__ wlo2,
-    int alo2, int aro2, __half* __restrict__ z2,
-    float* __restrict__ sl2, float* __restrict__ sr2,
+    __syncthreads();
+    zg_doset(Ah, Alo, part, tid, l, w, base, nrows, det, whi1, wlo1, al, alo1, ar, aro1, z1, sl1, sr1);
+    zg_doset(Ah, Alo, part, tid, l, w, base, nrows, det, whi2, wlo2, al, alo2, ar, aro2, z2, sl2, sr2);
+}
+
+__global__ __launch_bounds__(256, 2) void m_zgemm_dual(
+    const float* __restrict__ hA, int nA,
+    const u16* __restrict__ whiA, const u16* __restrict__ wloA, int aloA, int aroA,
+    __half* __restrict__ zA, float* __restrict__ slA, float* __restrict__ srA,
+    const float* __restrict__ hB, int nB,
+    const u16* __restrict__ whiB, const u16* __restrict__ wloB, int aloB, int aroB,
+    __half* __restrict__ zB, float* __restrict__ slB, float* __restrict__ srB,
     const void* __restrict__ al, const void* __restrict__ ar,
     const int* __restrict__ fl, const int* __restrict__ mfok)
 {
@@ -599,7 +674,17 @@
     __shared__ float part[2][4][64];
     const int det = *fl;
     const int tid = threadIdx.x, l = tid & 63, w = tid >> 6;
-    const int base = blockIdx.x * 64;
+    const int nblkA = (nA + 63) / 64;
+    const bool rb = (int)blockIdx.x >= nblkA;
+    const float* h = rb ? hB : hA;
+    const int nrows = rb ? nB : nA;
+    const u16* whi = rb ? whiB : whiA;
+    const u16* wlo = rb ? wloB : wloA;
+    const int aloff = rb ? aloB : aloA, aroff = rb ? aroB : aroA;
+    __half* z = rb ? zB : zA;
+    float* sl = rb ? slB : slA;
+    float* sr = rb ? srB : srA;
+    const int base = (rb ? blockIdx.x - nblkA : blockIdx.x) * 64;
     {
         int row = tid >> 2, q = tid & 3;
         int n = base + row, mi = row >> 4, r = row & 15;
@@ -623,78 +708,7 @@
         }
     }
     __syncthreads();
-    const int g = l >> 4, r = l & 15, wn0 = w * 32;
-    auto doSet = [&](const u16* whi, const u16* wlo, int aloff, int aroff,
-                     __half* z, float* sl, float* sr) {
-        bf16x8 breg[2][4];
-        #pragma unroll
-        for (int t = 0; t < 2; ++t)
-            #pragma unroll
-            for (int kk = 0; kk < 4; ++kk)
-                breg[t][kk] = *(const bf16x8*)(whi + ((size_t)((w * 2 + t) * 4 + kk) * 64 + l) * 8);
-        f32x4 acc[4][2];
-        #pragma unroll
-        for (int mi = 0; mi < 4; ++mi) { acc[mi][0] = (f32x4){0.f,0.f,0.f,0.f}; acc[mi][1] = (f32x4){0.f,0.f,0.f,0.f}; }
-        auto pass = [&](const short* AS) {
-            #pragma unroll
-            for (int kk = 0; kk < 4; ++kk) {
-                bf16x8 a[4];
-                #pragma unroll
-                for (int mi = 0; mi < 4; ++mi) a[mi] = *(const bf16x8*)&AS[((mi * 4 + kk) * 64 + l) * 8];
-                #pragma unroll
-                for (int mi = 0; mi < 4; ++mi) {
-                    acc[mi][0] = __builtin_amdgcn_mfma_f32_16x16x32_bf16(a[mi], breg[0][kk], acc[mi][0], 0, 0, 0);
-                    acc[mi][1] = __builtin_amdgcn_mfma_f32_16x16x32_bf16(a[mi], breg[1][kk], acc[mi][1], 0, 0, 0);
-                }
-            }
-        };
-        pass(Ah);
-        pass(Alo);
-        #pragma unroll
-        for (int t = 0; t < 2; ++t)
-            #pragma unroll
-            for (int kk = 0; kk < 4; ++kk)
-                breg[t][kk] = *(const bf16x8*)(wlo + ((size_t)((w * 2 + t) * 4 + kk) * 64 + l) * 8);
-        pass(Ah);
-        const float alv0 = gldf(al, (size_t)aloff + wn0 + r, det);
-        const float alv1 = gldf(al, (size_t)aloff + wn0 + 16 + r, det);
-        const float arv0 = gldf(ar, (size_t)aroff + wn0 + r, det);
-        const float arv1 = gldf(ar, (size_t)aroff + wn0 + 16 + r, det);
-        #pragma unroll
-        for (int mi = 0; mi < 4; ++mi)
-            #pragma unroll
-            for (int j = 0; j < 4; ++j) {
-                int row = base + mi * 16 + 4 * g + j;
-                float d0 = acc[mi][0][j], d1 = acc[mi][1][j];
-                if (row < nrows) {
-                    z[(size_t)row * 128 + wn0 + r]      = __float2half_rn(d0);
-                    z[(size_t)row * 128 + wn0 + 16 + r] = __float2half_rn(d1);
-                }
-                float pl = d0 * alv0 + d1 * alv1;
-                float pr = d0 * arv0 + d1 * arv1;
-                #pragma unroll
-                for (int m2 = 1; m2 < 16; m2 <<= 1) {
-                    pl += __shfl_xor(pl, m2, 64);
-                    pr += __shfl_xor(pr, m2, 64);
-                }
-                if (r == 0) {
-                    part[0][w][mi * 16 + 4 * g + j] = pl;
-                    part[1][w][mi * 16 + 4 * g + j] = pr;
-                }
-            }
-        __syncthreads();
-        if (tid < 128) {
-            int which = tid >> 6, t = tid & 63;
-            int n2 = base + t;
-            if (n2 < nrows) {
-                float s = part[which][0][t] + part[which][1][t] + part[which][2][t] + part[which][3][t];
-                (which ? sr : sl)[n2] = s;
-            }
-        }
-        __syncthreads();
-    };
-    doSet(whi1, wlo1, alo1, aro1, z1, sl1, sr1);
-    doSet(whi2, wlo2, alo2, aro2, z2, sl2, sr2);
+    zg_doset(Ah, Alo, part, tid, l, w, base, nrows, det, whi, wlo, al, aloff, ar, aroff, z, sl, sr);
 }
 
 __global__ __launch_bounds__(256, 2) void m_gatefeat(
@@ -766,18 +780,28 @@
     const int g = l >> 4, r = l & 15, wn0 = w * 32;
     const float bv0 = gldf(bias, wn0 + r, det);
     const float bv1 = gldf(bias, wn0 + 16 + r, det);
+    auto recon = [&](int nloc, int colg) -> float {
+        int c = colg >> 3, jj = colg & 7;
+        int slot = (((nloc >> 4) * 8 + (c >> 2)) * 4 + (c & 3)) * 16 + (nloc & 15);
+        return bf2f((u16)Ah[slot * 8 + jj]) + bf2f((u16)Alo[slot * 8 + jj]);
+    };
     #pragma unroll
     for (int mi = 0; mi < 4; ++mi)
         #pragma unroll
         for (int j = 0; j < 4; ++j) {
-            int row = base + mi * 16 + 4 * g + j;
+            int nloc = mi * 16 + 4 * g + j;
+            int row = base + nloc;
             if (row < nrows) {
                 size_t o0 = (size_t)row * 128 + wn0 + r;
                 size_t o1 = o0 + 16;
+                float h0a = recon(nloc, wn0 + r);
+                float h0b = recon(nloc, wn0 + 16 + r);
+                float h1a = recon(nloc, 128 + wn0 + r);
+                float h1b = recon(nloc, 128 + wn0 + 16 + r);
                 float ga  = sigm(acc[mi][0][j] + bv0);
                 float gb2 = sigm(acc[mi][1][j] + bv1);
-                feat[o0] = ga  * h0[o0] + (1.f - ga)  * h1[o0];
-                feat[o1] = gb2 * h0[o1] + (1.f - gb2) * h1[o1];
+                feat[o0] = ga  * h0a + (1.f - ga)  * h1a;
+                feat[o1] = gb2 * h0b + (1.f - gb2) * h1b;
             }
         }
 }
@@ -932,6 +956,139 @@
             beta[n2] = s * (float)mask[n2];
         }
     }
+}
+
+__global__ __launch_bounds__(256, 2) void m_lin(
+    const float* __restrict__ hsvn, const float* __restrict__ hall0,
+    const u16* __restrict__ whi1, const u16* __restrict__ wlo1,
+    const u16* __restrict__ whi2, const u16* __restrict__ wlo2,
+    const void* __restrict__ lb,
+    const int* __restrict__ fl, const int* __restrict__ mfok,
+    float* __restrict__ g2, int nrows)
+{
+    if (*mfok == 0) return;
+    __shared__ __align__(16) short Ah[2048 * 8];
+    __shared__ __align__(16) short Alo[2048 * 8];
+    const int det = *fl;
+    const int tid = threadIdx.x, l = tid & 63, w = tid >> 6;
+    const int base = blockIdx.x * 64;
+    {
+        int row = tid >> 2, q = tid & 3;
+        int n = base + row, mi = row >> 4, r = row & 15;
+        #pragma unroll
+        for (int i = 0; i < 8; ++i) {
+            int c = q + 4 * i, kk = c >> 2, g = c & 3;
+            int slot = ((mi * 8 + kk) * 4 + g) * 16 + r;
+            bf16x8 hv = {0,0,0,0,0,0,0,0}, lv = {0,0,0,0,0,0,0,0};
+            if (n < nrows) {
+                const float* sp = (c < 16) ? hsvn + (size_t)n * 128 + c * 8
+                                           : hall0 + (size_t)n * T_ * 128 + (c - 16) * 8;
+                #pragma unroll
+                for (int j = 0; j < 8; ++j) {
+                    float x = sp[j];
+                    u16 hb = f2bf(x);
+                    hv[j] = (short)hb;
+                    lv[j] = (short)f2bf(x - bf2f(hb));
+                }
+            }
+            *(bf16x8*)&Ah[slot * 8]  = hv;
+            *(bf16x8*)&Alo[slot * 8] = lv;
+        }
+    }
+    bf16x8 breg[2][8];
+    #pragma unroll
+    for (int t = 0; t < 2; ++t)
+        #pragma unroll
+        for (int kk = 0; kk < 8; ++kk)
+            breg[t][kk] = *(const bf16x8*)(whi1 + ((size_t)((w * 2 + t) * 8 + kk) * 64 + l) * 8);
+    __syncthreads();
+    f32x4 acc[4][2];
+    #pragma unroll
+    for (int mi = 0; mi < 4; ++mi) { acc[mi][0] = (f32x4){0.f,0.f,0.f,0.f}; acc[mi][1] = (f32x4){0.f,0.f,0.f,0.f}; }
+    auto pass1 = [&](const short* AS) {
+        #pragma unroll
+        for (int kk = 0; kk < 8; ++kk) {
+            bf16x8 a[4];
+            #pragma unroll
+            for (int mi = 0; mi < 4; ++mi) a[mi] = *(const bf16x8*)&AS[((mi * 8 + kk) * 64 + l) * 8];
+            #pragma unroll
+            for (int mi = 0; mi < 4; ++mi) {
+                acc[mi][0] = __builtin_amdgcn_mfma_f32_16x16x32_bf16(a[mi], breg[0][kk], acc[mi][0], 0, 0, 0);
+                acc[mi][1] = __builtin_amdgcn_mfma_f32_16x16x32_bf16(a[mi], breg[1][kk], acc[mi][1], 0, 0, 0);
+            }
+        }
+    };
+    pass1(Ah);
+    pass1(Alo);
+    #pragma unroll
+    for (int t = 0; t < 2; ++t)
+        #pragma unroll
+        for (int kk = 0; kk < 8; ++kk)
+            breg[t][kk] = *(const bf16x8*)(wlo1 + ((size_t)((w * 2 + t) * 8 + kk) * 64 + l) * 8);
+    pass1(Ah);
+    __syncthreads();
+    {
+        const int g = l >> 4, r = l & 15, wn0 = w * 32;
+        #pragma unroll
+        for (int mi = 0; mi < 4; ++mi)
+            #pragma unroll
+            for (int j = 0; j < 4; ++j) {
+                int nloc = mi * 16 + 4 * g + j;
+                int rr = nloc & 15, mi2 = nloc >> 4;
+                #pragma unroll
+                for (int hh = 0; hh < 2; ++hh) {
+                    int col = wn0 + 16 * hh + r;
+                    float x = acc[mi][hh][j] + gldf(lb, col, det);
+                    int c = col >> 3, jj = col & 7;
+                    int slot = ((mi2 * 4 + (c >> 2)) * 4 + (c & 3)) * 16 + rr;
+                    u16 hb = f2bf(x);
+                    Ah[slot * 8 + jj]  = (short)hb;
+                    Alo[slot * 8 + jj] = (short)f2bf(x - bf2f(hb));
+                }
+            }
+    }
+    __syncthreads();
+    bf16x8 breg2[2][4];
+    #pragma unroll
+    for (int t = 0; t < 2; ++t)
+        #pragma unroll
+        for (int kk = 0; kk < 4; ++kk)
+            breg2[t][kk] = *(const bf16x8*)(whi2 + ((size_t)((w * 2 + t) * 4 + kk) * 64 + l) * 8);
+    f32x4 acc2[4][2];
+    #pragma unroll
+    for (int mi = 0; mi < 4; ++mi) { acc2[mi][0] = (f32x4){0.f,0.f,0.f,0.f}; acc2[mi][1] = (f32x4){0.f,0.f,0.f,0.f}; }
+    auto pass2 = [&](const short* AS) {
+        #pragma unroll
+        for (int kk = 0; kk < 4; ++kk) {
+            bf16x8 a[4];
+            #pragma unroll
+            for (int mi = 0; mi < 4; ++mi) a[mi] = *(const bf16x8*)&AS[((mi * 4 + kk) * 64 + l) * 8];
+            #pragma unroll
+            for (int mi = 0; mi < 4; ++mi) {
+                acc2[mi][0] = __builtin_amdgcn_mfma_f32_16x16x32_bf16(a[mi], breg2[0][kk], acc2[mi][0], 0, 0, 0);
+                acc2[mi][1] = __builtin_amdgcn_mfma_f32_16x16x32_bf16(a[mi], breg2[1][kk], acc2[mi][1], 0, 0, 0);
+            }
+        }
+    };
+    pass2(Ah);
+    pass2(Alo);
+    #pragma unroll
+    for (int t = 0; t < 2; ++t)
+        #pragma unroll
+        for (int kk = 0; kk < 4; ++kk)
+            breg2[t][kk] = *(const bf16x8*)(wlo2 + ((size_t)((w * 2 + t) * 4 + kk) * 64 + l) * 8);
+    pass2(Ah);
+    const int g = l >> 4, r = l & 15, wn0 = w * 32;
+    #pragma unroll
+    for (int mi = 0; mi < 4; ++mi)
+        #pragma unroll
+        for (int j = 0; j < 4; ++j) {
+            int row = base + mi * 16 + 4 * g + j;
+            if (row < nrows) {
+                g2[(size_t)row * 128 + wn0 + r]      = acc2[mi][0][j];
+                g2[(size_t)row * 128 + wn0 + 16 + r] = acc2[mi][1][j];
+            }
+        }
 }
 
 __global__ __launch_bounds__(512) void t_hi0(
@@ -1120,6 +1277,59 @@
         }
         __syncthreads();
     }
+}
+
+__global__ __launch_bounds__(128) void t_attn1n(
+    const void* __restrict__ item, const int* __restrict__ seq,
+    const int* __restrict__ alias, const int* __restrict__ maskp,
+    const float* __restrict__ feat, const void* __restrict__ xs,
+    const void* __restrict__ q,
+    const void* __restrict__ g, const void* __restrict__ bb,
+    const int* __restrict__ fl,
+    float* __restrict__ hall0, float* __restrict__ hsvn)
+{
+    __shared__ float hl[T_][129];
+    __shared__ float qs[128];
+    __shared__ float hs_s[T_];
+    __shared__ float red[128];
+    const int b = blockIdx.x, tid = threadIdx.x;
+    const int det = *fl;
+    const float x = gldf(xs, 0, det);
+    qs[tid] = gldf(q, tid, det);
+    for (int t = 0; t < T_; ++t) {
+        int bt = b * T_ + t;
+        float v = gldf(item, (size_t)seq[bt] * 128 + tid, det) * x
+                + feat[(size_t)alias[bt] * 128 + tid] * (float)maskp[bt];
+        hl[t][tid] = v;
+        hall0[(size_t)bt * 128 + tid] = v;
+    }
+    __syncthreads();
+    if (tid < T_) {
+        float a = 0.f;
+        for (int d = 0; d < 128; ++d) a += hl[tid][d] * qs[d];
+        hs_s[tid] = a;
+    }
+    __syncthreads();
+    float mx = -1e30f;
+    for (int t = 0; t < T_; ++t) mx = fmaxf(mx, hs_s[t]);
+    float ssum = 0.f;
+    for (int t = 0; t < T_; ++t) ssum += expf(hs_s[t] - mx);
+    float inv = 1.f / ssum;
+    __syncthreads();
+    if (tid < T_)
+        hs_s[tid] = expf(hs_s[tid] - mx) * inv * (float)maskp[b * T_ + tid];
+    __syncthreads();
+    float a = 0.f;
+    for (int t = 0; t < T_; ++t) a += hs_s[t] * hl[t][tid];
+    red[tid] = a; __syncthreads();
+    for (int o = 64; o > 0; o >>= 1) { if (tid < o) red[tid] += red[tid + o]; __syncthreads(); }
+    float mu = red[0] * (1.f / 128.f);
+    __syncthreads();
+    float dv = a - mu;
+    red[tid] = dv * dv; __syncthreads();
+    for (int o = 64; o > 0; o >>= 1) { if (tid < o) red[tid] += red[tid + o]; __syncthreads(); }
+    float rs = 1.f / sqrtf(red[0] * (1.f / 128.f) + 1e-8f);
+    hsvn[(size_t)b * 128 + tid] = dv * rs * gldf(g, tid, det) + gldf(bb, tid, det);
 }
 
 __global__ __launch_bounds__(128) void t_attn12(
@@ -1451,7 +1661,7 @@
     float* sl02p = HiB + 2 * (size_t)NI_;
     float* sr02s = sl02p + NC_;
     u16* wt2_hi = (u16*)HiA;
-    u16* wt2_lo = wt2_hi + (size_t)6144 * 8;
+    u16* wt2_lo = wt2_hi + (size_t)12288 * 8;
 
     auto WTS = [&](int l, int k) {
         int midx = (l == 0) ? k : ((k == 0) ? 4 : 5);
@@ -1498,39 +1708,48 @@
         k_binB<<<dim3(NBK_), dim3(512), 0, stream>>>(
             bstart, bcnt, binII, binCI, binCC, binIC,
             rpII, rpCI, rpCC, rpIC, csII, csCI, csCC, csIC);
-        m_hi0<<<dim3((NI_ + 63) / 64), dim3(256), 0, stream>>>(
-            item_emb, cate_emb, iid, icate, wt_hi, wt_lo, flagp, flagp + 1, hi0, NI_);
-        m_zgemm2<<<dim3((NI_ + 63) / 64), dim3(256), 0, stream>>>(
-            hi0, NI_,
-            wt_hi + WTS(0, 0), wt_lo + WTS(0, 0), VOFF(0, 0), VOFF(0, 0), zAh,  sAl,   sAr,
-            wt_hi + WTS(0, 3), wt_lo + WTS(0, 3), VOFF(0, 3), VOFF(0, 3), zA2h, sl03p, sr03s,
-            gat_al, gat_ar, flagp, flagp + 1);
+        m_hi0zg<<<dim3((NI_ + 63) / 64), dim3(256), 0, stream>>>(
+            item_emb, cate_emb, iid, icate,
+            wt_hi, wt_lo,
+            wt_hi + WTS(0, 0), wt_lo + WTS(0, 0), VOFF(0, 0), VOFF(0, 0),
+            wt_hi + WTS(0, 3), wt_lo + WTS(0, 3), VOFF(0, 3), VOFF(0, 3),
+            gat_al, gat_ar, flagp, flagp + 1,
+            hi0, zAh, sAl, sAr, zA2h, sl03p, sr03s, NI_);
         m_zgemm2<<<dim3((NC_ + 63) / 64), dim3(256), 0, stream>>>(
             hc0, NC_,
             wt_hi + WTS(0, 1), wt_lo + WTS(0, 1), VOFF(0, 1), VOFF(0, 1), zC2h, sCl,   sCr,
             wt_hi + WTS(0, 2), wt_lo + WTS(0, 2), VOFF(0, 2), VOFF(0, 2), zCh,  sl02p, sr02s,
             gat_al, gat_ar, flagp, flagp + 1);
-        t_gat_fused<<<dim3((NI_ + 3) / 4), dim3(256), 0, stream>>>(
+        t_gat2<<<dim3((NI_ + 3) / 4 + (NC_ + 3) / 4), dim3(256), 0, stream>>>(
             rpII, csII, sAl, sAr, (const __half2*)zAh,
             rpCI, csCI, sl02p, wars + 0, (const __half2*)zCh,
-            hi0, gat_b, VOFF(0, 0), VOFF(0, 2), flagp, HiA, NI_);
-        t_gat_fused<<<dim3((NC_ + 3) / 4), dim3(256), 0, stream>>>(
+            hi0, VOFF(0, 0), VOFF(0, 2), HiA,
             rpCC, csCC, sCl, sCr, (const __half2*)zC2h,
             rpIC, csIC, sl03p, wars + 128, (const __half2*)zA2h,
-            hc0, gat_b, VOFF(0, 1), VOFF(0, 3), flagp, HcA, NC_);
-        m_zgemm<<<dim3((NI_ + 63) / 64), dim3(256), 0, stream>>>(
-            HiA, NI_, wt_hi + WTS(1, 0), wt_lo + WTS(1, 0),
-            gat_al, VOFF(1, 0), gat_ar, VOFF(1, 0), flagp, flagp + 1, zAh, sAl, sAr);
-        m_zgemm<<<dim3((NC_ + 63) / 64), dim3(256), 0, stream>>>(
-            HcA, NC_, wt_hi + WTS(1, 2), wt_lo + WTS(1, 2),
-            gat_al, VOFF(1, 2), gat_ar, VOFF(1, 2), flagp, flagp + 1, zCh, sCl, sCr);
+            hc0, VOFF(0, 1), VOFF(0, 3), HcA,
+            gat_b, flagp);
+        m_zgemm_dual<<<dim3((NI_ + 63) / 64 + (NC_ + 63) / 64), dim3(256), 0, stream>>>(
+            HiA, NI_, wt_hi + WTS(1, 0), wt_lo + WTS(1, 0), VOFF(1, 0), VOFF(1, 0), zAh, sAl, sAr,
+            HcA, NC_, wt_hi + WTS(1, 2), wt_lo + WTS(1, 2), VOFF(1, 2), VOFF(1, 2), zCh, sCl, sCr,
+            gat_al, gat_ar, flagp, flagp + 1);
         t_gat_fused<<<dim3((NI_ + 3) / 4), dim3(256), 0, stream>>>(
             rpII, csII, sAl, sAr, (const __half2*)zAh,
             rpCI, csCI, sCl, wars + 256, (const __half2*)zCh,
             HiA, gat_b, VOFF(1, 0), VOFF(1, 2), flagp, HiB, NI_);
-        k_prepw3<<<dim3(24), dim3(256), 0, stream>>>(w_1, glu1_w, flagp, wt2_hi, wt2_lo);
+        k_prepw3<<<dim3(48), dim3(256), 0, stream>>>(w_1, glu1_w, lin_w, glu2_w, flagp, wt2_hi, wt2_lo);
         m_gatefeat<<<dim3((NI_ + 63) / 64), dim3(256), 0, stream>>>(
             hi0, HiB, wt_hi + (size_t)4096 * 8, wt_lo + (size_t)4096 * 8, Wg1_b, flagp, flagp + 1, feat, NI_);
+        t_attn1n<<<dim3(B_), dim3(128), 0, stream>>>(
+            item_emb, seq, alias, mask, feat, x_s, q, ln1_g, ln1_b, flagp, hall0, hsvn);
+        m_lin<<<dim3((B_ + 63) / 64), dim3(256), 0, stream>>>(
+            hsvn, hall0,
+            wt2_hi + (size_t)6144 * 8, wt2_lo + (size_t)6144 * 8,
+            wt2_hi + (size_t)10240 * 8, wt2_lo + (size_t)10240 * 8,
+            lin_b, flagp, flagp + 1, g2b, B_);
+        m_nhglu<<<dim3((B_ * T_ + 63) / 64), dim3(256), 0, stream>>>(
+            pos_emb, hall0, wt2_hi, wt2_lo,
+            wt2_hi + (size_t)4096 * 8, wt2_lo + (size_t)4096 * 8,
+            glu1_b, g2b, w_2, mask, flagp, flagp + 1, betab, B_ * T_);
     } else {
         s_hc0<<<GRL((long)NC_ * 128), dim3(256), 0, stream>>>(cate_emb, cid, flagp, hc0);
         t_hi0<<<dim3(768), dim3(512), 0, stream>>>(item_emb, cate_emb, iid, icate, W_pos, flagp, hi0, NI_);
@@ -1553,21 +1772,14 @@
         t_zgemm<<<dim3(1024), dim3(512), 0, stream>>>(HiA, NI_, gat_W, WOFF(1, 2), gat_al, VOFF(1, 2), gat_ar, VOFF(1, 2), flagp, zAh, sAl, sAr);
         seg(sCl, sAr, src_ci, dst_ci, ECI_, NI_, zCh, HiB);
         t_gatefeat<<<dim3(768), dim3(512), 0, stream>>>(hi0, HiB, Wg1_w, Wg1_b, flagp, feat, NI_);
-    }
-
-    t_attn12<<<dim3(B_), dim3(128), 0, stream>>>(
-        item_emb, seq, alias, mask, feat, x_s, q,
-        ln1_g, ln1_b, lin_w, lin_b, glu2_w, flagp, hall0, g2b);
-    if (mf) {
-        m_nhglu<<<dim3((B_ * T_ + 63) / 64), dim3(256), 0, stream>>>(
-            pos_emb, hall0, wt2_hi, wt2_lo,
-            wt2_hi + (size_t)4096 * 8, wt2_lo + (size_t)4096 * 8,
-            glu1_b, g2b, w_2, mask, flagp, flagp + 1, betab, B_ * T_);
-    } else {
+        t_attn12<<<dim3(B_), dim3(128), 0, stream>>>(
+            item_emb, seq, alias, mask, feat, x_s, q,
+            ln1_g, ln1_b, lin_w, lin_b, glu2_w, flagp, hall0, g2b);
         int grid = (B_ * T_ + 15) / 16; if (grid > 1024) grid = 1024;
         t_nh<<<dim3(grid), dim3(512), 0, stream>>>(pos_emb, hall0, w_1, flagp, nh, B_ * T_);
         t_glu_beta<<<dim3(grid), dim3(512), 0, stream>>>(nh, glu1_w, glu1_b, g2b, w_2, mask, flagp, betab, B_ * T_);
     }
+
     t_sel<<<dim3(B_), dim3(128), 0, stream>>>(hall0, betab, ln2_g, ln2_b, feat, lasti, y_s, flagp, hallf, fenmu, outf);
     t_cos<<<dim3(B_), dim3(256), 0, stream>>>(hallf, fenmu, outf + (size_t)B_ * 128);
 }
```

New measurement: 793.6 us. -7.8%, faster.
